# Optimization experiments

Measured on AMD Instinct MI355X. Metric: run time of the kernel, lower is better.

## Reference

```python
import jax, jax.numpy as jnp
import numpy as np
import math

L = 4      # layers / experts
AD = 512   # agent dim per layer
D = 512    # wsi_size / model dim
T = 64     # num_tokens
N = 4096   # WSI patches
NC = 2
PROJ = 256 # cosine gate projection dim
HID = 4 * D
CAP = math.ceil(T / L)  # top-1, capacity_factor=1.0
EPS = 1e-5
AUX_W = 0.01


def layer_norm(x, g, b):
    x32 = x.astype(jnp.float32)
    mu = x32.mean(-1, keepdims=True)
    var = x32.var(-1, keepdims=True)
    return ((x32 - mu) * jax.lax.rsqrt(var + EPS) * g + b).astype(x.dtype)


def mha(q_in, kv_in, w_qkv, b_qkv, w_out, b_out, n_heads):
    # torch nn.MultiheadAttention, unbatched (len, embed) inputs
    E = q_in.shape[-1]
    hd = E // n_heads
    wq, wk, wv = jnp.split(w_qkv, 3, axis=0)
    bq, bk, bv = jnp.split(b_qkv, 3)
    q = (q_in @ wq.T + bq).reshape(-1, n_heads, hd)
    k = (kv_in @ wk.T + bk).reshape(-1, n_heads, hd)
    v = (kv_in @ wv.T + bv).reshape(-1, n_heads, hd)
    scale = float(1.0 / np.sqrt(hd))
    attn = jax.nn.softmax(jnp.einsum('thd,shd->hts', q, k) * scale, axis=-1)
    out = jnp.einsum('hts,shd->thd', attn, v).reshape(-1, E)
    return out @ w_out.T + b_out


def moe_top1(x, proj_w, sim_mat, temp, w1, b1, w2, b2):
    # tutel cosine top-1 gate (fp32), capacity-limited batch-prioritized dispatch
    E = w1.shape[0]
    xf = x.astype(jnp.float32)
    p = xf @ proj_w                                             # [T, PROJ]
    p = p / (jnp.linalg.norm(p, axis=-1, keepdims=True) + 1e-8)
    s = sim_mat / (jnp.linalg.norm(sim_mat, axis=0, keepdims=True) + 1e-8)
    scale = jnp.exp(jnp.minimum(temp, jnp.log(jnp.float32(100.0))))
    logits = (p @ s) * scale                                    # [T, E]
    scores = jax.nn.softmax(logits, axis=-1)
    expert = jnp.argmax(logits, axis=-1)                        # [T]
    gate = jnp.take_along_axis(scores, expert[:, None], axis=1)[:, 0]
    # batch prioritized routing: higher-gate tokens claim capacity slots first
    order = jnp.argsort(-gate)
    oh = jax.nn.one_hot(expert[order], E, dtype=jnp.int32)
    pos_s = jnp.sum(jnp.cumsum(oh, axis=0) * oh, axis=1) - 1    # slot within expert
    inv = jnp.argsort(order)
    pos = pos_s[inv]
    keep = pos < CAP
    safe_pos = jnp.where(keep, pos, 0)
    # dispatch -> grouped expert FFN -> combine
    buf = jnp.zeros((E, CAP, x.shape[-1]), x.dtype)
    buf = buf.at[expert, safe_pos].add(jnp.where(keep[:, None], x, 0.0))
    h = jax.nn.gelu(jnp.einsum('ecd,edh->ech', buf, w1) + b1[:, None, :], approximate=False)
    y = jnp.einsum('ech,ehd->ecd', h, w2) + b2[:, None, :]
    out = y[expert, safe_pos] * (gate * keep)[:, None].astype(x.dtype)
    # load-balancing aux loss (top-1)
    me = scores.mean(0)
    ce = jax.nn.one_hot(expert, E, dtype=jnp.float32).mean(0)
    l_aux = jnp.sum(me * ce) * E
    return out, l_aux


def reference(share_feature, fet_tokens, ind_ln1_g, ind_ln1_b, ind_ln2_g, ind_ln2_b,
              ind_qkv_w, ind_qkv_b, ind_out_w, ind_out_b, ind_mlp_w, ind_mlp_b,
              gate_proj_w, gate_sim, gate_temp, exp_w1, exp_b1, exp_w2, exp_b2,
              gsa_ln1_g, gsa_ln1_b, gsa_qkv_w, gsa_qkv_b, gsa_out_w, gsa_out_b,
              gsa_ln2_g, gsa_ln2_b, gsa_fc_w, gsa_fc_b, gsa_proj_w, gsa_proj_b,
              butter_w, butter_b, cls_w, cls_b):
    cur = jnp.zeros((T, D), share_feature.dtype)
    feature1 = jnp.zeros((L, T, D), share_feature.dtype)
    aux = jnp.zeros((1,), jnp.float32)
    for i in range(L):  # small fixed per-layer loop (structurally distinct params)
        seg = share_feature[:, i * AD:(i + 1) * AD]
        sf = layer_norm(seg, ind_ln1_g[i], ind_ln1_b[i])
        tok = layer_norm(fet_tokens[i], ind_ln2_g[i], ind_ln2_b[i])
        attn_out = mha(tok, sf, ind_qkv_w[i], ind_qkv_b[i], ind_out_w[i], ind_out_b[i], AD)
        qf = attn_out @ ind_mlp_w[i].T + ind_mlp_b[i]   # [T, D]
        mo, la = moe_top1(qf, gate_proj_w, gate_sim, gate_temp, exp_w1, exp_b1, exp_w2, exp_b2)
        cur = cur + mo
        aux = aux + la * AUX_W
        feature1 = feature1.at[i].set(cur)
    cur = cur / L
    # GatedSFAttentionBlock (8 heads self-attn + QuickGELU MLP, pre-LN residual)
    x1 = layer_norm(cur, gsa_ln1_g, gsa_ln1_b)
    x = cur + mha(x1, x1, gsa_qkv_w, gsa_qkv_b, gsa_out_w, gsa_out_b, D // 64)
    x2 = layer_norm(x, gsa_ln2_g, gsa_ln2_b)
    h = x2 @ gsa_fc_w.T + gsa_fc_b
    h = h * jax.nn.sigmoid(1.702 * h)  # QuickGELU
    gated = x + (h @ gsa_proj_w.T + gsa_proj_b)
    # OutputBlock
    hb = (gated @ butter_w.T + butter_b).reshape(1, -1)  # [1, T*256]
    logits = hb @ cls_w.T + cls_b                        # [1, NC]
    Y_hat = jnp.argmax(logits, axis=1, keepdims=True)
    hazards = jax.nn.sigmoid(logits)
    feature2 = jnp.zeros((L, T, D), share_feature.dtype)
    feature2_pre = jnp.zeros((L, 1, NC), share_feature.dtype)
    return (logits, hazards, Y_hat, aux, feature1, feature2, feature2_pre)


def setup_inputs() -> dict:
    key = jax.random.key(0)
    ks = iter(jax.random.split(key, 40))
    def rn(shape, scale=0.02):
        return scale * jax.random.normal(next(ks), shape, dtype=jnp.float32)
    return dict(
        share_feature=jax.random.normal(next(ks), (N, L * AD), dtype=jnp.float32),
        fet_tokens=rn((L, T, AD), AD ** -0.5),
        ind_ln1_g=jnp.ones((L, AD)), ind_ln1_b=jnp.zeros((L, AD)),
        ind_ln2_g=jnp.ones((L, AD)), ind_ln2_b=jnp.zeros((L, AD)),
        ind_qkv_w=rn((L, 3 * AD, AD)), ind_qkv_b=jnp.zeros((L, 3 * AD)),
        ind_out_w=rn((L, AD, AD)), ind_out_b=jnp.zeros((L, AD)),
        ind_mlp_w=rn((L, D, AD)), ind_mlp_b=jnp.zeros((L, D)),
        gate_proj_w=rn((D, PROJ)), gate_sim=rn((PROJ, L)),
        gate_temp=jnp.asarray(np.log(10.0), jnp.float32),
        exp_w1=rn((L, D, HID)), exp_b1=jnp.zeros((L, HID)),
        exp_w2=rn((L, HID, D)), exp_b2=jnp.zeros((L, D)),
        gsa_ln1_g=jnp.ones((D,)), gsa_ln1_b=jnp.zeros((D,)),
        gsa_qkv_w=rn((3 * D, D)), gsa_qkv_b=jnp.zeros((3 * D,)),
        gsa_out_w=rn((D, D)), gsa_out_b=jnp.zeros((D,)),
        gsa_ln2_g=jnp.ones((D,)), gsa_ln2_b=jnp.zeros((D,)),
        gsa_fc_w=rn((4 * D, D)), gsa_fc_b=jnp.zeros((4 * D,)),
        gsa_proj_w=rn((D, 4 * D)), gsa_proj_b=jnp.zeros((D,)),
        butter_w=rn((256, D)), butter_b=jnp.zeros((256,)),
        cls_w=rn((NC, T * 256)), cls_b=jnp.zeros((NC,)),
    )
```

## Files before the change

### kernel.cpp

```cpp
#include <hip/hip_runtime.h>
#include <math.h>

#define LNUM 4
#define ADIM 512
#define TTOK 64
#define NSEQ 4096
#define HIDE 2048
#define CAPE 16
#define EPSV 1e-5f

typedef __bf16 bf16;
typedef bf16 bf16x8 __attribute__((ext_vector_type(8)));
typedef float f32x4 __attribute__((ext_vector_type(4)));

#define OFF_BUF   0
#define OFF_SSUM  (OFF_BUF  + 131072)
#define OFF_CNT   (OFF_SSUM + 16)
#define OFF_Q     (OFF_CNT  + 16)
#define OFF_AP    (OFF_Q    + 131072)
#define OFF_QF    (OFF_AP   + 131072)
#define OFF_P     (OFF_QF   + 131072)
#define OFF_QKV3  (OFF_P    + 65536)
#define OFF_XB    (OFF_QKV3 + 98304)
#define OFF_HROW  (OFF_XB   + 32768)
#define OFF_GTD   (OFF_HROW + 131072)
#define OFF_HB    (OFF_GTD  + 32768)
#define ZERO_N    (OFF_HB   + 16384)
#define OFF_KT    ZERO_N
#define OFF_VT    (OFF_KT   + LNUM*512*NSEQ)
#define OFF_AO    (OFF_VT   + LNUM*512*NSEQ)
#define OFF_GATE  (OFF_AO   + 131072)
#define OFF_EXP   (OFF_GATE + 256)
#define OFF_POS   (OFF_EXP  + 256)
#define OFF_KEEP  (OFF_POS  + 256)
#define OFF_HEXP  (OFF_KEEP + 256)
#define OFF_CUR   (OFF_HEXP + LNUM*4*CAPE*HIDE)
#define OFF_AO2   (OFF_CUR  + TTOK*512)
#define OFF_AH    (OFF_AO2  + TTOK*512)
#define OFF_AL    (OFF_AH + LNUM*NSEQ*256)
#define OFF_WH    (OFF_AL + LNUM*NSEQ*256)
#define OFF_WL    (OFF_WH + LNUM*1024*256)
#define OFF_YEXP  OFF_AH

#define O_F1   6
#define O_F2   (6 + LNUM*TTOK*512)
#define O_F2P  (O_F2 + LNUM*TTOK*512)

__device__ __forceinline__ float wave_sum(float v) {
#pragma unroll
  for (int o = 32; o > 0; o >>= 1) v += __shfl_down(v, o, 64);
  return v;
}
__device__ __forceinline__ float wave_sum_all(float v) {
#pragma unroll
  for (int o = 32; o > 0; o >>= 1) v += __shfl_xor(v, o, 64);
  return v;
}
__device__ __forceinline__ float block_sum256(float v) {
  __shared__ float r[4];
  v = wave_sum(v);
  int wid = threadIdx.x >> 6, lane = threadIdx.x & 63;
  if (lane == 0) r[wid] = v;
  __syncthreads();
  float s = r[0] + r[1] + r[2] + r[3];
  __syncthreads();
  return s;
}

__global__ void k_zero(float* __restrict__ p, int n) {
  int i = blockIdx.x * 256 + threadIdx.x;
  if (i < n) p[i] = 0.f;
}

__global__ __launch_bounds__(64) void k_cvt_a(const float* __restrict__ SF,
      const float* __restrict__ G, const float* __restrict__ Bta,
      bf16* __restrict__ AH, bf16* __restrict__ AL) {
  int row = blockIdx.x;
  int l = row >> 12, m = row & 4095;
  int lane = threadIdx.x;
  const float* src = SF + (size_t)m * (LNUM * ADIM) + l * ADIM;
  float4 a = *(const float4*)(src + lane * 8);
  float4 b = *(const float4*)(src + lane * 8 + 4);
  float sum = (a.x + a.y) + (a.z + a.w) + (b.x + b.y) + (b.z + b.w);
  float sq = a.x*a.x + a.y*a.y + a.z*a.z + a.w*a.w + b.x*b.x + b.y*b.y + b.z*b.z + b.w*b.w;
  sum = wave_sum_all(sum); sq = wave_sum_all(sq);
  float mu = sum * (1.f / 512.f);
  float rs = rsqrtf(sq * (1.f / 512.f) - mu * mu + EPSV);
  float4 g0 = *(const float4*)(G + l * 512 + lane * 8);
  float4 g1 = *(const float4*)(G + l * 512 + lane * 8 + 4);
  float4 c0 = *(const float4*)(Bta + l * 512 + lane * 8);
  float4 c1 = *(const float4*)(Bta + l * 512 + lane * 8 + 4);
  float x[8];
  x[0] = (a.x - mu) * rs * g0.x + c0.x;  x[1] = (a.y - mu) * rs * g0.y + c0.y;
  x[2] = (a.z - mu) * rs * g0.z + c0.z;  x[3] = (a.w - mu) * rs * g0.w + c0.w;
  x[4] = (b.x - mu) * rs * g1.x + c1.x;  x[5] = (b.y - mu) * rs * g1.y + c1.y;
  x[6] = (b.z - mu) * rs * g1.z + c1.z;  x[7] = (b.w - mu) * rs * g1.w + c1.w;
  bf16x8 vh, vl;
#pragma unroll
  for (int j = 0; j < 8; j++) {
    bf16 h = (bf16)x[j];
    vh[j] = h;
    vl[j] = (bf16)(x[j] - (float)h);
  }
  *(bf16x8*)(AH + (size_t)row * 512 + lane * 8) = vh;
  *(bf16x8*)(AL + (size_t)row * 512 + lane * 8) = vl;
}

__global__ __launch_bounds__(64) void k_cvt_w(const float* __restrict__ Wqkv,
      bf16* __restrict__ WH, bf16* __restrict__ WL) {
  int row = blockIdx.x;
  int l = row >> 10, r = row & 1023;
  int lane = threadIdx.x;
  const float* src = Wqkv + (size_t)l * 1536 * 512 + (size_t)(512 + r) * 512 + lane * 8;
  float4 a = *(const float4*)(src);
  float4 b = *(const float4*)(src + 4);
  float x[8] = {a.x, a.y, a.z, a.w, b.x, b.y, b.z, b.w};
  bf16x8 vh, vl;
#pragma unroll
  for (int j = 0; j < 8; j++) {
    bf16 h = (bf16)x[j];
    vh[j] = h;
    vl[j] = (bf16)(x[j] - (float)h);
  }
  *(bf16x8*)(WH + (size_t)row * 512 + lane * 8) = vh;
  *(bf16x8*)(WL + (size_t)row * 512 + lane * 8) = vl;
}

#define KVP 40
__global__ __launch_bounds__(256) void k_mfma_kv(
      const bf16* __restrict__ AH, const bf16* __restrict__ AL,
      const bf16* __restrict__ WH, const bf16* __restrict__ WL,
      const float* __restrict__ Bqkv,
      float* __restrict__ KT, float* __restrict__ VT) {
  __shared__ bf16 sAh[128*KVP], sAl[128*KVP], sWh[128*KVP], sWl[128*KVP];
  int l = blockIdx.z;
  int m0 = blockIdx.x * 128, n0 = blockIdx.y * 128;
  int tid = threadIdx.x;
  int lane = tid & 63;
  int w = tid >> 6;
  int wm = w >> 1, wn = w & 1;
  const bf16* gAh = AH + ((size_t)l * 4096 + m0) * 512;
  const bf16* gAl = AL + ((size_t)l * 4096 + m0) * 512;
  const bf16* gWh = WH + ((size_t)l * 1024 + n0) * 512;
  const bf16* gWl = WL + ((size_t)l * 1024 + n0) * 512;
  int ch0 = tid * 2, ch1 = tid * 2 + 1;
  int r0 = ch0 >> 2, q0 = (ch0 & 3) * 8;
  int r1 = ch1 >> 2, q1 = (ch1 & 3) * 8;
  int fr = lane & 15, fq = (lane >> 4) * 8;
  f32x4 acc[4][4] = {};
  for (int k0 = 0; k0 < 512; k0 += 32) {
    *(bf16x8*)&sAh[r0*KVP + q0] = *(const bf16x8*)&gAh[(size_t)r0*512 + k0 + q0];
    *(bf16x8*)&sAh[r1*KVP + q1] = *(const bf16x8*)&gAh[(size_t)r1*512 + k0 + q1];
    *(bf16x8*)&sAl[r0*KVP + q0] = *(const bf16x8*)&gAl[(size_t)r0*512 + k0 + q0];
    *(bf16x8*)&sAl[r1*KVP + q1] = *(const bf16x8*)&gAl[(size_t)r1*512 + k0 + q1];
    *(bf16x8*)&sWh[r0*KVP + q0] = *(const bf16x8*)&gWh[(size_t)r0*512 + k0 + q0];
    *(bf16x8*)&sWh[r1*KVP + q1] = *(const bf16x8*)&gWh[(size_t)r1*512 + k0 + q1];
    *(bf16x8*)&sWl[r0*KVP + q0] = *(const bf16x8*)&gWl[(size_t)r0*512 + k0 + q0];
    *(bf16x8*)&sWl[r1*KVP + q1] = *(const bf16x8*)&gWl[(size_t)r1*512 + k0 + q1];
    __syncthreads();
    bf16x8 ah[4], al[4], bh[4], bl[4];
#pragma unroll
    for (int i = 0; i < 4; i++) {
      ah[i] = *(const bf16x8*)&sAh[(wm*64 + i*16 + fr)*KVP + fq];
      al[i] = *(const bf16x8*)&sAl[(wm*64 + i*16 + fr)*KVP + fq];
      bh[i] = *(const bf16x8*)&sWh[(wn*64 + i*16 + fr)*KVP + fq];
      bl[i] = *(const bf16x8*)&sWl[(wn*64 + i*16 + fr)*KVP + fq];
    }
#pragma unroll
    for (int i = 0; i < 4; i++)
#pragma unroll
      for (int j = 0; j < 4; j++) {
        acc[i][j] = __builtin_amdgcn_mfma_f32_16x16x32_bf16(ah[i], bh[j], acc[i][j], 0, 0, 0);
        acc[i][j] = __builtin_amdgcn_mfma_f32_16x16x32_bf16(ah[i], bl[j], acc[i][j], 0, 0, 0);
        acc[i][j] = __builtin_amdgcn_mfma_f32_16x16x32_bf16(al[i], bh[j], acc[i][j], 0, 0, 0);
      }
    __syncthreads();
  }
#pragma unroll
  for (int j = 0; j < 4; j++) {
    int n = n0 + wn*64 + j*16 + fr;
    float bias = Bqkv[l * 1536 + 512 + n];
    float* base = (n < 512) ? (KT + ((size_t)(l*512 + n)) * 4096)
                            : (VT + ((size_t)(l*512 + n - 512)) * 4096);
#pragma unroll
    for (int i = 0; i < 4; i++) {
      int mb = m0 + wm*64 + i*16 + (lane >> 4) * 4;
      float4 o = make_float4(acc[i][j][0] + bias, acc[i][j][1] + bias,
                             acc[i][j][2] + bias, acc[i][j][3] + bias);
      *(float4*)(base + mb) = o;
    }
  }
}

__global__ __launch_bounds__(64) void k_ln(const float* __restrict__ IN,
      const float* __restrict__ G, const float* __restrict__ B,
      float* __restrict__ OUT, int gstride) {
  int t = blockIdx.x, l = blockIdx.y;
  int row = l * 64 + t;
  int lane = threadIdx.x;
  const float* x = IN + (size_t)row * 512 + lane * 8;
  float4 a = ((const float4*)x)[0], b = ((const float4*)x)[1];
  float sum = (a.x + a.y) + (a.z + a.w) + (b.x + b.y) + (b.z + b.w);
  float sq = a.x*a.x + a.y*a.y + a.z*a.z + a.w*a.w + b.x*b.x + b.y*b.y + b.z*b.z + b.w*b.w;
  sum = wave_sum_all(sum); sq = wave_sum_all(sq);
  float mu = sum * (1.f / 512.f);
  float rs = rsqrtf(sq * (1.f / 512.f) - mu * mu + EPSV);
  const float* gp = G + l * gstride + lane * 8;
  const float* bp = B + l * gstride + lane * 8;
  float4 g0 = ((const float4*)gp)[0], g1 = ((const float4*)gp)[1];
  float4 c0 = ((const float4*)bp)[0], c1 = ((const float4*)bp)[1];
  float4 o0, o1;
  o0.x = (a.x - mu) * rs * g0.x + c0.x;  o0.y = (a.y - mu) * rs * g0.y + c0.y;
  o0.z = (a.z - mu) * rs * g0.z + c0.z;  o0.w = (a.w - mu) * rs * g0.w + c0.w;
  o1.x = (b.x - mu) * rs * g1.x + c1.x;  o1.y = (b.y - mu) * rs * g1.y + c1.y;
  o1.z = (b.z - mu) * rs * g1.z + c1.z;  o1.w = (b.w - mu) * rs * g1.w + c1.w;
  float* op = OUT + (size_t)row * 512 + lane * 8;
  ((float4*)op)[0] = o0; ((float4*)op)[1] = o1;
}

__global__ __launch_bounds__(256) void k_gemm64(
      const float* __restrict__ IN, const float* __restrict__ W,
      const float* __restrict__ BIAS, const float* __restrict__ RES,
      float* __restrict__ OUT, int K, int N, long wl, int bl, int act) {
  int l = blockIdx.z;
  int n0 = blockIdx.x * 64;
  bool split = (gridDim.y > 1);
  int kcBeg = blockIdx.y * 128;
  int kcEnd = split ? kcBeg + 128 : K;
  const float* INl = IN + (size_t)l * 64 * K;
  const float* Wl  = W + (size_t)l * wl;
  float* OUTl = OUT + (size_t)l * 64 * N;
  __shared__ float sA[64][68], sB[64][68];
  int tid = threadIdx.x;
  int tx = tid & 15, ty = tid >> 4;
  float acc[4][4];
  if (blockIdx.y == 0) {
#pragma unroll
    for (int j = 0; j < 4; j++) {
      float bv = BIAS ? BIAS[bl * l + n0 + tx*4 + j] : 0.f;
#pragma unroll
      for (int i = 0; i < 4; i++)
        acc[i][j] = bv + (RES ? RES[((size_t)l*64 + ty*4 + i) * N + n0 + tx*4 + j] : 0.f);
    }
  } else {
#pragma unroll
    for (int i = 0; i < 4; i++)
#pragma unroll
      for (int j = 0; j < 4; j++) acc[i][j] = 0.f;
  }
  for (int kc = kcBeg; kc < kcEnd; kc += 64) {
    for (int i = tid; i < 1024; i += 256) {
      int r = i >> 4;
      int kq = i & 15;
      float4 av = *(const float4*)(INl + (size_t)r * K + kc + kq*4);
      sA[kq*4+0][r] = av.x; sA[kq*4+1][r] = av.y; sA[kq*4+2][r] = av.z; sA[kq*4+3][r] = av.w;
      float4 bv = *(const float4*)(Wl + (size_t)(n0 + r) * K + kc + kq*4);
      sB[kq*4+0][r] = bv.x; sB[kq*4+1][r] = bv.y; sB[kq*4+2][r] = bv.z; sB[kq*4+3][r] = bv.w;
    }
    __syncthreads();
#pragma unroll 8
    for (int kk = 0; kk < 64; kk++) {
      float4 a4 = *(const float4*)&sA[kk][ty*4];
      float4 b4 = *(const float4*)&sB[kk][tx*4];
      float a[4] = {a4.x,a4.y,a4.z,a4.w}, b[4] = {b4.x,b4.y,b4.z,b4.w};
#pragma unroll
      for (int i = 0; i < 4; i++)
#pragma unroll
        for (int j = 0; j < 4; j++) acc[i][j] = fmaf(a[i], b[j], acc[i][j]);
    }
    __syncthreads();
  }
  if (split) {
#pragma unroll
    for (int i = 0; i < 4; i++)
#pragma unroll
      for (int j = 0; j < 4; j++)
        atomicAdd(&OUTl[(size_t)(ty*4+i) * N + n0 + tx*4 + j], acc[i][j]);
  } else {
#pragma unroll
    for (int i = 0; i < 4; i++)
#pragma unroll
      for (int j = 0; j < 4; j++) {
        float o = acc[i][j];
        if (act == 1) o = o / (1.f + __expf(-1.702f * o));
        OUTl[(size_t)(ty*4+i) * N + n0 + tx*4 + j] = o;
      }
  }
}

__global__ __launch_bounds__(256) void k_gemm64t(
      const float* __restrict__ IN, const float* __restrict__ W,
      float* __restrict__ OUT, int K, int N) {
  int l = blockIdx.z;
  int n0 = blockIdx.x * 64;
  int kc0 = blockIdx.y * 128;
  const float* INl = IN + (size_t)l * 64 * K;
  float* OUTl = OUT + (size_t)l * 64 * N;
  __shared__ float sA[64][68], sB[64][68];
  int tid = threadIdx.x;
  int tx = tid & 15, ty = tid >> 4;
  float acc[4][4] = {};
  for (int kc = kc0; kc < kc0 + 128; kc += 64) {
    for (int i = tid; i < 1024; i += 256) {
      int r = i >> 4;
      int kq = i & 15;
      float4 av = *(const float4*)(INl + (size_t)r * K + kc + kq*4);
      sA[kq*4+0][r] = av.x; sA[kq*4+1][r] = av.y; sA[kq*4+2][r] = av.z; sA[kq*4+3][r] = av.w;
      float4 bv = *(const float4*)(W + (size_t)(kc + r) * N + n0 + kq*4);
      *(float4*)&sB[r][kq*4] = bv;
    }
    __syncthreads();
#pragma unroll 8
    for (int kk = 0; kk < 64; kk++) {
      float4 a4 = *(const float4*)&sA[kk][ty*4];
      float4 b4 = *(const float4*)&sB[kk][tx*4];
      float a[4] = {a4.x,a4.y,a4.z,a4.w}, b[4] = {b4.x,b4.y,b4.z,b4.w};
#pragma unroll
      for (int i = 0; i < 4; i++)
#pragma unroll
        for (int j = 0; j < 4; j++) acc[i][j] = fmaf(a[i], b[j], acc[i][j]);
    }
    __syncthreads();
  }
#pragma unroll
  for (int i = 0; i < 4; i++)
#pragma unroll
    for (int j = 0; j < 4; j++)
      atomicAdd(&OUTl[(size_t)(ty*4+i) * N + n0 + tx*4 + j], acc[i][j]);
}

__global__ __launch_bounds__(256) void k_attn(const float* __restrict__ KT, const float* __restrict__ VT,
      const float* __restrict__ Q, float* __restrict__ AO) {
  int h = blockIdx.x, l = blockIdx.y;
  int tid = threadIdx.x;
  int w = tid >> 6, lane = tid & 63;
  __shared__ float2 sacc[4][8][66];
  __shared__ float wmx[4], wmn[4];
  size_t base = ((size_t)(l * 512 + h)) * 4096 + w * 1024;
  float kv[16], vv[16];
#pragma unroll
  for (int c = 0; c < 4; c++) {
    *(float4*)&kv[c*4] = *(const float4*)(KT + base + c * 256 + lane * 4);
    *(float4*)&vv[c*4] = *(const float4*)(VT + base + c * 256 + lane * 4);
  }
  float mx = kv[0], mn = kv[0];
#pragma unroll
  for (int i = 1; i < 16; i++) { mx = fmaxf(mx, kv[i]); mn = fminf(mn, kv[i]); }
#pragma unroll
  for (int o = 32; o > 0; o >>= 1) {
    mx = fmaxf(mx, __shfl_xor(mx, o, 64));
    mn = fminf(mn, __shfl_xor(mn, o, 64));
  }
  if (lane == 0) { wmx[w] = mx; wmn[w] = mn; }
  __syncthreads();
  float km = fmaxf(fmaxf(wmx[0], wmx[1]), fmaxf(wmx[2], wmx[3]));
  float kn = fminf(fminf(wmn[0], wmn[1]), fminf(wmn[2], wmn[3]));
  float q_own = Q[((size_t)l * TTOK + lane) * 512 + h];
  float m_own = (q_own >= 0.f) ? q_own * km : q_own * kn;
  int rt = tid >> 5, rj = tid & 31;
  for (int cc = 0; cc < 8; cc++) {
    for (int tt = 0; tt < 8; tt++) {
      int t = cc * 8 + tt;
      float qt = __shfl(q_own, t, 64);
      float mt = __shfl(m_own, t, 64);
      float den = 0.f, num = 0.f;
#pragma unroll
      for (int i = 0; i < 16; i++) {
        float e = __expf(fmaf(qt, kv[i], -mt));
        den += e;
        num = fmaf(e, vv[i], num);
      }
      sacc[w][tt][lane] = make_float2(den, num);
    }
    __syncthreads();
    float2 a = make_float2(0.f, 0.f);
#pragma unroll
    for (int g = 0; g < 4; g++)
#pragma unroll
      for (int s2 = 0; s2 < 2; s2++) {
        float2 v = sacc[g][rt][rj + 32 * s2];
        a.x += v.x; a.y += v.y;
      }
#pragma unroll
    for (int o = 16; o > 0; o >>= 1) {
      a.x += __shfl_down(a.x, o, 32);
      a.y += __shfl_down(a.y, o, 32);
    }
    if (rj == 0) {
      int t = cc * 8 + rt;
      AO[((size_t)l * TTOK + t) * 512 + h] = a.y / a.x;
    }
    __syncthreads();
  }
}

__global__ __launch_bounds__(256) void k_moe_gate(const float* __restrict__ P,
      const float* __restrict__ SIM, const float* __restrict__ TEMP,
      const float* __restrict__ QF,
      float* __restrict__ gate, int* __restrict__ expert,
      int* __restrict__ pos, int* __restrict__ keep,
      float* __restrict__ ssum, int* __restrict__ cnt, float* __restrict__ buf) {
  int l = blockIdx.x;
  int tid = threadIdx.x;
  int t = tid >> 2, q = tid & 3;
  __shared__ float score_s[4][64];
  __shared__ float g_s[64];
  __shared__ int e_s[64], keep_s[64], pos_s[64];
  const float* prow = P + ((size_t)(l * 64 + t)) * 256 + q * 64;
  float ss = 0.f, le[4] = {}, ne[4] = {};
  for (int j = 0; j < 64; j++) {
    float pv = prow[j];
    ss = fmaf(pv, pv, ss);
    float4 s4 = *(const float4*)(SIM + (size_t)(q * 64 + j) * 4);
    le[0] = fmaf(pv, s4.x, le[0]); le[1] = fmaf(pv, s4.y, le[1]);
    le[2] = fmaf(pv, s4.z, le[2]); le[3] = fmaf(pv, s4.w, le[3]);
    ne[0] = fmaf(s4.x, s4.x, ne[0]); ne[1] = fmaf(s4.y, s4.y, ne[1]);
    ne[2] = fmaf(s4.z, s4.z, ne[2]); ne[3] = fmaf(s4.w, s4.w, ne[3]);
  }
#pragma unroll
  for (int o = 2; o > 0; o >>= 1) {
    ss += __shfl_xor(ss, o, 4);
#pragma unroll
    for (int e = 0; e < 4; e++) { le[e] += __shfl_xor(le[e], o, 4); ne[e] += __shfl_xor(ne[e], o, 4); }
  }
  if (q == 0) {
    float invp = 1.f / (sqrtf(ss) + 1e-8f);
    float scale = __expf(fminf(TEMP[0], 4.6051701859880914f));
    float lg[4];
#pragma unroll
    for (int e = 0; e < 4; e++) lg[e] = le[e] * invp / (sqrtf(ne[e]) + 1e-8f) * scale;
    int best = 0; float bv = lg[0];
    if (lg[1] > bv) { best = 1; bv = lg[1]; }
    if (lg[2] > bv) { best = 2; bv = lg[2]; }
    if (lg[3] > bv) { best = 3; bv = lg[3]; }
    float mx = fmaxf(fmaxf(lg[0], lg[1]), fmaxf(lg[2], lg[3]));
    float e0 = __expf(lg[0]-mx), e1 = __expf(lg[1]-mx), e2 = __expf(lg[2]-mx), e3 = __expf(lg[3]-mx);
    float inv = 1.f / (e0 + e1 + e2 + e3);
    score_s[0][t] = e0*inv; score_s[1][t] = e1*inv; score_s[2][t] = e2*inv; score_s[3][t] = e3*inv;
    float sb = score_s[best][t];
    g_s[t] = sb; e_s[t] = best;
    gate[l * TTOK + t] = sb;
    expert[l * TTOK + t] = best;
  }
  __syncthreads();
  if (tid < 64) {
    float gt = g_s[tid]; int et = e_s[tid];
    int p = 0;
    for (int u = 0; u < 64; u++)
      if (e_s[u] == et && (g_s[u] > gt || (g_s[u] == gt && u < tid))) p++;
    pos_s[tid] = p; keep_s[tid] = (p < CAPE) ? 1 : 0;
    pos[l * TTOK + tid] = p;
    keep[l * TTOK + tid] = (p < CAPE) ? 1 : 0;
  } else if (tid < 68) {
    int e = tid - 64;
    float s = 0.f; int c = 0;
    for (int u = 0; u < 64; u++) { s += score_s[e][u]; c += (e_s[u] == e); }
    ssum[l * 4 + e] = s;
    cnt[l * 4 + e] = c;
  }
  __syncthreads();
  int which = tid >> 7, idx = tid & 127;
  for (int tb = 0; tb < 64; tb += 2) {
    int tt = tb + which;
    if (keep_s[tt]) {
      float4* dst = (float4*)(buf + (((size_t)(l * 4 + e_s[tt])) * CAPE + pos_s[tt]) * 512);
      dst[idx] = ((const float4*)(QF + ((size_t)l * TTOK + tt) * 512))[idx];
    }
  }
}

__global__ __launch_bounds__(256) void k_moe_h(const float* __restrict__ buf, const float* __restrict__ W1,
      const float* __restrict__ B1, float* __restrict__ H) {
  int le = blockIdx.y;
  int e = le & 3;
  int col = blockIdx.x * 256 + threadIdx.x;
  const float* act = buf + (size_t)le * 16 * 512;
  const float* wp = W1 + (size_t)e * 512 * HIDE + col;
  float acc[16];
#pragma unroll
  for (int c = 0; c < 16; c++) acc[c] = 0.f;
  for (int k0 = 0; k0 < 512; k0 += 4) {
    float4 a[16];
#pragma unroll
    for (int c = 0; c < 16; c++) a[c] = *(const float4*)(act + c * 512 + k0);
#pragma unroll
    for (int j = 0; j < 4; j++) {
      float wv = wp[(size_t)(k0 + j) * HIDE];
#pragma unroll
      for (int c = 0; c < 16; c++) acc[c] = fmaf(((const float*)&a[c])[j], wv, acc[c]);
    }
  }
  float bias = B1[e * HIDE + col];
  float* outp = H + (size_t)le * 16 * HIDE + col;
#pragma unroll
  for (int c = 0; c < 16; c++) {
    float v = acc[c] + bias;
    outp[(size_t)c * HIDE] = 0.5f * v * (1.f + erff(v * 0.70710678118654752f));
  }
}

__global__ __launch_bounds__(256) void k_moe_y(const float* __restrict__ H, const float* __restrict__ W2,
      const float* __restrict__ B2, float* __restrict__ Y) {
  int le = blockIdx.y;
  int e = le & 3;
  int cl = threadIdx.x & 63, kq = threadIdx.x >> 6;
  int col = blockIdx.x * 64 + cl;
  const float* act = H + (size_t)le * 16 * HIDE + kq * 512;
  const float* wp = W2 + (size_t)e * HIDE * 512 + (size_t)(kq * 512) * 512 + col;
  float acc[16];
#pragma unroll
  for (int c = 0; c < 16; c++) acc[c] = 0.f;
  for (int k0 = 0; k0 < 512; k0 += 4) {
    float4 a[16];
#pragma unroll
    for (int c = 0; c < 16; c++) a[c] = *(const float4*)(act + c * HIDE + k0);
#pragma unroll
    for (int j = 0; j < 4; j++) {
      float wv = wp[(size_t)(k0 + j) * 512];
#pragma unroll
      for (int c = 0; c < 16; c++) acc[c] = fmaf(((const float*)&a[c])[j], wv, acc[c]);
    }
  }
  __shared__ float sacc[4][16][64];
#pragma unroll
  for (int c = 0; c < 16; c++) sacc[kq][c][cl] = acc[c];
  __syncthreads();
  if (kq == 0) {
    float bias = B2[e * 512 + col];
#pragma unroll
    for (int c = 0; c < 16; c++) {
      float tot = sacc[0][c][cl] + sacc[1][c][cl] + sacc[2][c][cl] + sacc[3][c][cl] + bias;
      Y[(size_t)le * 16 * 512 + (size_t)c * 512 + col] = tot;
    }
  }
}

__global__ __launch_bounds__(512) void k_combine(const float* __restrict__ Y, const int* __restrict__ expert,
      const int* __restrict__ pos, const int* __restrict__ keep, const float* __restrict__ gate,
      float* __restrict__ f1, float* __restrict__ f2, float* __restrict__ cur) {
  int t = blockIdx.x;
  int d = threadIdx.x;
  float acc = 0.f;
#pragma unroll
  for (int l = 0; l < LNUM; l++) {
    int idx = l * TTOK + t;
    float v = 0.f;
    if (keep[idx]) {
      int e = expert[idx], p = pos[idx];
      v = Y[(((size_t)(l * 4 + e)) * CAPE + p) * 512 + d] * gate[idx];
    }
    acc += v;
    f1[((size_t)l * TTOK + t) * 512 + d] = acc;
    f2[((size_t)l * TTOK + t) * 512 + d] = 0.f;
  }
  cur[(size_t)t * 512 + d] = acc * 0.25f;
}

__global__ __launch_bounds__(256) void k_gsa_attn(const float* __restrict__ QKV3, float* __restrict__ AO2) {
  int h = blockIdx.x;
  __shared__ float qh[64][65], kh[64][65], vh[64][65];
  __shared__ float ps[4][64];
  for (int i = threadIdx.x; i < 4096; i += 256) {
    int t = i >> 6, d = i & 63;
    qh[t][d] = QKV3[(size_t)t * 1536 + h * 64 + d];
    kh[t][d] = QKV3[(size_t)t * 1536 + 512 + h * 64 + d];
    vh[t][d] = QKV3[(size_t)t * 1536 + 1024 + h * 64 + d];
  }
  __syncthreads();
  int w = threadIdx.x >> 6, lane = threadIdx.x & 63;
  for (int tt = 0; tt < 16; tt++) {
    int t = w * 16 + tt;
    float acc = 0.f;
#pragma unroll 8
    for (int d = 0; d < 64; d++) acc = fmaf(qh[t][d], kh[lane][d], acc);
    acc *= 0.125f;
    float m = acc;
#pragma unroll
    for (int o = 32; o > 0; o >>= 1) m = fmaxf(m, __shfl_xor(m, o, 64));
    float e = __expf(acc - m);
    float den = e;
#pragma unroll
    for (int o = 32; o > 0; o >>= 1) den += __shfl_xor(den, o, 64);
    ps[w][lane] = e / den;
    __syncthreads();
    float o2 = 0.f;
#pragma unroll 8
    for (int s = 0; s < 64; s++) o2 = fmaf(ps[w][s], vh[s][lane], o2);
    AO2[(size_t)t * 512 + h * 64 + lane] = o2;
    __syncthreads();
  }
}

__global__ __launch_bounds__(256) void k_final(const float* __restrict__ HB,
      const float* __restrict__ CW, const float* __restrict__ CB,
      const float* __restrict__ ssum, const int* __restrict__ cnt,
      float* __restrict__ out) {
  int tid = threadIdx.x;
  float p0 = 0.f, p1 = 0.f;
  for (int i = tid; i < 16384; i += 256) {
    float h = HB[i];
    p0 = fmaf(h, CW[i], p0);
    p1 = fmaf(h, CW[16384 + i], p1);
  }
  p0 = block_sum256(p0);
  p1 = block_sum256(p1);
  if (tid == 0) {
    float l0 = p0 + CB[0], l1 = p1 + CB[1];
    out[0] = l0; out[1] = l1;
    out[2] = 1.f / (1.f + __expf(-l0));
    out[3] = 1.f / (1.f + __expf(-l1));
    out[4] = (l1 > l0) ? 1.f : 0.f;
    float aux = 0.f;
    for (int i = 0; i < 16; i++) aux += (ssum[i] * (1.f / 64.f)) * ((float)cnt[i] * (1.f / 64.f));
    out[5] = aux * 4.f * 0.01f;
  }
  if (tid < 8) out[O_F2P + tid] = 0.f;
}

extern "C" void kernel_launch(void* const* d_in, const int* in_sizes, int n_in,
                              void* d_out, int out_size, void* d_ws, size_t ws_size,
                              hipStream_t stream) {
  const float* SF    = (const float*)d_in[0];
  const float* TOK   = (const float*)d_in[1];
  const float* LN1G  = (const float*)d_in[2];
  const float* LN1B  = (const float*)d_in[3];
  const float* LN2G  = (const float*)d_in[4];
  const float* LN2B  = (const float*)d_in[5];
  const float* QKVW  = (const float*)d_in[6];
  const float* QKVB  = (const float*)d_in[7];
  const float* OUTW  = (const float*)d_in[8];
  const float* OUTB  = (const float*)d_in[9];
  const float* MLPW  = (const float*)d_in[10];
  const float* MLPB  = (const float*)d_in[11];
  const float* GPW   = (const float*)d_in[12];
  const float* GSIM  = (const float*)d_in[13];
  const float* GTMP  = (const float*)d_in[14];
  const float* EW1   = (const float*)d_in[15];
  const float* EB1   = (const float*)d_in[16];
  const float* EW2   = (const float*)d_in[17];
  const float* EB2   = (const float*)d_in[18];
  const float* GL1G  = (const float*)d_in[19];
  const float* GL1B  = (const float*)d_in[20];
  const float* GQKVW = (const float*)d_in[21];
  const float* GQKVB = (const float*)d_in[22];
  const float* GOUTW = (const float*)d_in[23];
  const float* GOUTB = (const float*)d_in[24];
  const float* GL2G  = (const float*)d_in[25];
  const float* GL2B  = (const float*)d_in[26];
  const float* GFCW  = (const float*)d_in[27];
  const float* GFCB  = (const float*)d_in[28];
  const float* GPJW  = (const float*)d_in[29];
  const float* GPJB  = (const float*)d_in[30];
  const float* BTW   = (const float*)d_in[31];
  const float* BTB   = (const float*)d_in[32];
  const float* CLW   = (const float*)d_in[33];
  const float* CLB   = (const float*)d_in[34];

  float* ws  = (float*)d_ws;
  float* out = (float*)d_out;

  float* BUF  = ws + OFF_BUF;
  float* SSUM = ws + OFF_SSUM;
  int*   CNT  = (int*)(ws + OFF_CNT);
  float* Q    = ws + OFF_Q;
  float* AP   = ws + OFF_AP;
  float* QF   = ws + OFF_QF;
  float* P    = ws + OFF_P;
  float* QKV3 = ws + OFF_QKV3;
  float* XB   = ws + OFF_XB;
  float* HROW = ws + OFF_HROW;
  float* GTD  = ws + OFF_GTD;
  float* HBB  = ws + OFF_HB;
  float* KT   = ws + OFF_KT;
  float* VT   = ws + OFF_VT;
  float* AOSH = ws + OFF_AO;
  float* GATE = ws + OFF_GATE;
  int*   EXPI = (int*)(ws + OFF_EXP);
  int*   POSI = (int*)(ws + OFF_POS);
  int*   KEEPI= (int*)(ws + OFF_KEEP);
  float* HEXP = ws + OFF_HEXP;
  float* CUR  = ws + OFF_CUR;
  float* AO2  = ws + OFF_AO2;
  bf16*  AH   = (bf16*)(ws + OFF_AH);
  bf16*  AL   = (bf16*)(ws + OFF_AL);
  bf16*  WH   = (bf16*)(ws + OFF_WH);
  bf16*  WL   = (bf16*)(ws + OFF_WL);
  float* YEXP = ws + OFF_YEXP;

  k_zero<<<(ZERO_N + 255) / 256, 256, 0, stream>>>(ws, ZERO_N);
  k_cvt_a<<<LNUM * NSEQ, 64, 0, stream>>>(SF, LN1G, LN1B, AH, AL);
  k_cvt_w<<<LNUM * 1024, 64, 0, stream>>>(QKVW, WH, WL);
  k_mfma_kv<<<dim3(32, 8, LNUM), 256, 0, stream>>>(AH, AL, WH, WL, QKVB, KT, VT);
  k_ln<<<dim3(TTOK, LNUM), 64, 0, stream>>>(TOK, LN2G, LN2B, AOSH, 512);
  k_gemm64<<<dim3(8, 4, LNUM), 256, 0, stream>>>(AOSH, QKVW, QKVB, nullptr, Q, 512, 512, 1536L*512, 1536, 0);
  k_attn<<<dim3(512, LNUM), 256, 0, stream>>>(KT, VT, Q, AOSH);
  k_gemm64<<<dim3(8, 4, LNUM), 256, 0, stream>>>(AOSH, OUTW, OUTB, nullptr, AP, 512, 512, 512L*512, 512, 0);
  k_gemm64<<<dim3(8, 4, LNUM), 256, 0, stream>>>(AP, MLPW, MLPB, nullptr, QF, 512, 512, 512L*512, 512, 0);
  k_gemm64t<<<dim3(4, 4, LNUM), 256, 0, stream>>>(QF, GPW, P, 512, 256);
  k_moe_gate<<<LNUM, 256, 0, stream>>>(P, GSIM, GTMP, QF, GATE, EXPI, POSI, KEEPI, SSUM, CNT, BUF);
  k_moe_h<<<dim3(8, 16), 256, 0, stream>>>(BUF, EW1, EB1, HEXP);
  k_moe_y<<<dim3(8, 16), 256, 0, stream>>>(HEXP, EW2, EB2, YEXP);
  k_combine<<<TTOK, 512, 0, stream>>>(YEXP, EXPI, POSI, KEEPI, GATE, out + O_F1, out + O_F2, CUR);
  k_ln<<<dim3(TTOK, 1), 64, 0, stream>>>(CUR, GL1G, GL1B, AOSH, 0);
  k_gemm64<<<dim3(24, 4, 1), 256, 0, stream>>>(AOSH, GQKVW, GQKVB, nullptr, QKV3, 512, 1536, 0, 0, 0);
  k_gsa_attn<<<8, 256, 0, stream>>>(QKV3, AO2);
  k_gemm64<<<dim3(8, 4, 1), 256, 0, stream>>>(AO2, GOUTW, GOUTB, CUR, XB, 512, 512, 0, 0, 0);
  k_ln<<<dim3(TTOK, 1), 64, 0, stream>>>(XB, GL2G, GL2B, AOSH, 0);
  k_gemm64<<<dim3(32, 1, 1), 256, 0, stream>>>(AOSH, GFCW, GFCB, nullptr, HROW, 512, 2048, 0, 0, 1);
  k_gemm64<<<dim3(8, 16, 1), 256, 0, stream>>>(HROW, GPJW, GPJB, XB, GTD, 2048, 512, 0, 0, 0);
  k_gemm64<<<dim3(4, 4, 1), 256, 0, stream>>>(GTD, BTW, BTB, nullptr, HBB, 512, 256, 0, 0, 0);
  k_final<<<1, 256, 0, stream>>>(HBB, CLW, CLB, SSUM, CNT, out);
}
```

Baseline: 792.8 us.

## Merge many small kernel launches into persistent megakernels with grid barriers

After: 982.0 us. 23.9% more time.

```diff
diff --git a/kernel.cpp b/kernel.cpp
--- a/kernel.cpp
+++ b/kernel.cpp
@@ -8,15 +8,23 @@
 #define HIDE 2048
 #define CAPE 16
 #define EPSV 1e-5f
+#define LOG2E 1.44269504088896340736f
 
 typedef __bf16 bf16;
 typedef bf16 bf16x8 __attribute__((ext_vector_type(8)));
 typedef float f32x4 __attribute__((ext_vector_type(4)));
 
+#if __has_builtin(__builtin_amdgcn_exp2f)
+#define EXP2F(x) __builtin_amdgcn_exp2f(x)
+#else
+#define EXP2F(x) __expf(0.69314718055994530942f * (x))
+#endif
+
 #define OFF_BUF   0
-#define OFF_SSUM  (OFF_BUF  + 131072)
-#define OFF_CNT   (OFF_SSUM + 16)
-#define OFF_Q     (OFF_CNT  + 16)
+#define OFF_SSUM  131072
+#define OFF_CNT   131088
+#define OFF_BAR   131104
+#define OFF_Q     131120
 #define OFF_AP    (OFF_Q    + 131072)
 #define OFF_QF    (OFF_AP   + 131072)
 #define OFF_P     (OFF_QF   + 131072)
@@ -26,6 +34,7 @@
 #define OFF_GTD   (OFF_HROW + 131072)
 #define OFF_HB    (OFF_GTD  + 32768)
 #define ZERO_N    (OFF_HB   + 16384)
+#define NZB       ((ZERO_N + 255) / 256)
 #define OFF_KT    ZERO_N
 #define OFF_VT    (OFF_KT   + LNUM*512*NSEQ)
 #define OFF_AO    (OFF_VT   + LNUM*512*NSEQ)
@@ -67,180 +76,53 @@
   return s;
 }
 
-__global__ void k_zero(float* __restrict__ p, int n) {
-  int i = blockIdx.x * 256 + threadIdx.x;
-  if (i < n) p[i] = 0.f;
-}
-
-__global__ __launch_bounds__(64) void k_cvt_a(const float* __restrict__ SF,
-      const float* __restrict__ G, const float* __restrict__ Bta,
-      bf16* __restrict__ AH, bf16* __restrict__ AL) {
-  int row = blockIdx.x;
-  int l = row >> 12, m = row & 4095;
-  int lane = threadIdx.x;
-  const float* src = SF + (size_t)m * (LNUM * ADIM) + l * ADIM;
-  float4 a = *(const float4*)(src + lane * 8);
-  float4 b = *(const float4*)(src + lane * 8 + 4);
+__device__ __forceinline__ void gsync(unsigned* bar, unsigned target) {
+  __syncthreads();
+  if (threadIdx.x == 0) {
+    __threadfence();
+    atomicAdd(bar, 1u);
+    while (__hip_atomic_load(bar, __ATOMIC_RELAXED, __HIP_MEMORY_SCOPE_AGENT) < target)
+      __builtin_amdgcn_s_sleep(2);
+  }
+  __syncthreads();
+  __threadfence();
+}
+
+__device__ __forceinline__ void ln_row(const float* __restrict__ x,
+      const float* __restrict__ G, const float* __restrict__ B, float* __restrict__ o) {
+  int lane = threadIdx.x & 63;
+  float4 a = *(const float4*)(x + lane * 8);
+  float4 b = *(const float4*)(x + lane * 8 + 4);
   float sum = (a.x + a.y) + (a.z + a.w) + (b.x + b.y) + (b.z + b.w);
   float sq = a.x*a.x + a.y*a.y + a.z*a.z + a.w*a.w + b.x*b.x + b.y*b.y + b.z*b.z + b.w*b.w;
   sum = wave_sum_all(sum); sq = wave_sum_all(sq);
   float mu = sum * (1.f / 512.f);
   float rs = rsqrtf(sq * (1.f / 512.f) - mu * mu + EPSV);
-  float4 g0 = *(const float4*)(G + l * 512 + lane * 8);
-  float4 g1 = *(const float4*)(G + l * 512 + lane * 8 + 4);
-  float4 c0 = *(const float4*)(Bta + l * 512 + lane * 8);
-  float4 c1 = *(const float4*)(Bta + l * 512 + lane * 8 + 4);
-  float x[8];
-  x[0] = (a.x - mu) * rs * g0.x + c0.x;  x[1] = (a.y - mu) * rs * g0.y + c0.y;
-  x[2] = (a.z - mu) * rs * g0.z + c0.z;  x[3] = (a.w - mu) * rs * g0.w + c0.w;
-  x[4] = (b.x - mu) * rs * g1.x + c1.x;  x[5] = (b.y - mu) * rs * g1.y + c1.y;
-  x[6] = (b.z - mu) * rs * g1.z + c1.z;  x[7] = (b.w - mu) * rs * g1.w + c1.w;
-  bf16x8 vh, vl;
-#pragma unroll
-  for (int j = 0; j < 8; j++) {
-    bf16 h = (bf16)x[j];
-    vh[j] = h;
-    vl[j] = (bf16)(x[j] - (float)h);
-  }
-  *(bf16x8*)(AH + (size_t)row * 512 + lane * 8) = vh;
-  *(bf16x8*)(AL + (size_t)row * 512 + lane * 8) = vl;
-}
-
-__global__ __launch_bounds__(64) void k_cvt_w(const float* __restrict__ Wqkv,
-      bf16* __restrict__ WH, bf16* __restrict__ WL) {
-  int row = blockIdx.x;
-  int l = row >> 10, r = row & 1023;
-  int lane = threadIdx.x;
-  const float* src = Wqkv + (size_t)l * 1536 * 512 + (size_t)(512 + r) * 512 + lane * 8;
-  float4 a = *(const float4*)(src);
-  float4 b = *(const float4*)(src + 4);
-  float x[8] = {a.x, a.y, a.z, a.w, b.x, b.y, b.z, b.w};
-  bf16x8 vh, vl;
-#pragma unroll
-  for (int j = 0; j < 8; j++) {
-    bf16 h = (bf16)x[j];
-    vh[j] = h;
-    vl[j] = (bf16)(x[j] - (float)h);
-  }
-  *(bf16x8*)(WH + (size_t)row * 512 + lane * 8) = vh;
-  *(bf16x8*)(WL + (size_t)row * 512 + lane * 8) = vl;
-}
-
-#define KVP 40
-__global__ __launch_bounds__(256) void k_mfma_kv(
-      const bf16* __restrict__ AH, const bf16* __restrict__ AL,
-      const bf16* __restrict__ WH, const bf16* __restrict__ WL,
-      const float* __restrict__ Bqkv,
-      float* __restrict__ KT, float* __restrict__ VT) {
-  __shared__ bf16 sAh[128*KVP], sAl[128*KVP], sWh[128*KVP], sWl[128*KVP];
-  int l = blockIdx.z;
-  int m0 = blockIdx.x * 128, n0 = blockIdx.y * 128;
-  int tid = threadIdx.x;
-  int lane = tid & 63;
-  int w = tid >> 6;
-  int wm = w >> 1, wn = w & 1;
-  const bf16* gAh = AH + ((size_t)l * 4096 + m0) * 512;
-  const bf16* gAl = AL + ((size_t)l * 4096 + m0) * 512;
-  const bf16* gWh = WH + ((size_t)l * 1024 + n0) * 512;
-  const bf16* gWl = WL + ((size_t)l * 1024 + n0) * 512;
-  int ch0 = tid * 2, ch1 = tid * 2 + 1;
-  int r0 = ch0 >> 2, q0 = (ch0 & 3) * 8;
-  int r1 = ch1 >> 2, q1 = (ch1 & 3) * 8;
-  int fr = lane & 15, fq = (lane >> 4) * 8;
-  f32x4 acc[4][4] = {};
-  for (int k0 = 0; k0 < 512; k0 += 32) {
-    *(bf16x8*)&sAh[r0*KVP + q0] = *(const bf16x8*)&gAh[(size_t)r0*512 + k0 + q0];
-    *(bf16x8*)&sAh[r1*KVP + q1] = *(const bf16x8*)&gAh[(size_t)r1*512 + k0 + q1];
-    *(bf16x8*)&sAl[r0*KVP + q0] = *(const bf16x8*)&gAl[(size_t)r0*512 + k0 + q0];
-    *(bf16x8*)&sAl[r1*KVP + q1] = *(const bf16x8*)&gAl[(size_t)r1*512 + k0 + q1];
-    *(bf16x8*)&sWh[r0*KVP + q0] = *(const bf16x8*)&gWh[(size_t)r0*512 + k0 + q0];
-    *(bf16x8*)&sWh[r1*KVP + q1] = *(const bf16x8*)&gWh[(size_t)r1*512 + k0 + q1];
-    *(bf16x8*)&sWl[r0*KVP + q0] = *(const bf16x8*)&gWl[(size_t)r0*512 + k0 + q0];
-    *(bf16x8*)&sWl[r1*KVP + q1] = *(const bf16x8*)&gWl[(size_t)r1*512 + k0 + q1];
-    __syncthreads();
-    bf16x8 ah[4], al[4], bh[4], bl[4];
-#pragma unroll
-    for (int i = 0; i < 4; i++) {
-      ah[i] = *(const bf16x8*)&sAh[(wm*64 + i*16 + fr)*KVP + fq];
-      al[i] = *(const bf16x8*)&sAl[(wm*64 + i*16 + fr)*KVP + fq];
-      bh[i] = *(const bf16x8*)&sWh[(wn*64 + i*16 + fr)*KVP + fq];
-      bl[i] = *(const bf16x8*)&sWl[(wn*64 + i*16 + fr)*KVP + fq];
-    }
-#pragma unroll
-    for (int i = 0; i < 4; i++)
-#pragma unroll
-      for (int j = 0; j < 4; j++) {
-        acc[i][j] = __builtin_amdgcn_mfma_f32_16x16x32_bf16(ah[i], bh[j], acc[i][j], 0, 0, 0);
-        acc[i][j] = __builtin_amdgcn_mfma_f32_16x16x32_bf16(ah[i], bl[j], acc[i][j], 0, 0, 0);
-        acc[i][j] = __builtin_amdgcn_mfma_f32_16x16x32_bf16(al[i], bh[j], acc[i][j], 0, 0, 0);
-      }
-    __syncthreads();
-  }
-#pragma unroll
-  for (int j = 0; j < 4; j++) {
-    int n = n0 + wn*64 + j*16 + fr;
-    float bias = Bqkv[l * 1536 + 512 + n];
-    float* base = (n < 512) ? (KT + ((size_t)(l*512 + n)) * 4096)
-                            : (VT + ((size_t)(l*512 + n - 512)) * 4096);
-#pragma unroll
-    for (int i = 0; i < 4; i++) {
-      int mb = m0 + wm*64 + i*16 + (lane >> 4) * 4;
-      float4 o = make_float4(acc[i][j][0] + bias, acc[i][j][1] + bias,
-                             acc[i][j][2] + bias, acc[i][j][3] + bias);
-      *(float4*)(base + mb) = o;
-    }
-  }
-}
-
-__global__ __launch_bounds__(64) void k_ln(const float* __restrict__ IN,
-      const float* __restrict__ G, const float* __restrict__ B,
-      float* __restrict__ OUT, int gstride) {
-  int t = blockIdx.x, l = blockIdx.y;
-  int row = l * 64 + t;
-  int lane = threadIdx.x;
-  const float* x = IN + (size_t)row * 512 + lane * 8;
-  float4 a = ((const float4*)x)[0], b = ((const float4*)x)[1];
-  float sum = (a.x + a.y) + (a.z + a.w) + (b.x + b.y) + (b.z + b.w);
-  float sq = a.x*a.x + a.y*a.y + a.z*a.z + a.w*a.w + b.x*b.x + b.y*b.y + b.z*b.z + b.w*b.w;
-  sum = wave_sum_all(sum); sq = wave_sum_all(sq);
-  float mu = sum * (1.f / 512.f);
-  float rs = rsqrtf(sq * (1.f / 512.f) - mu * mu + EPSV);
-  const float* gp = G + l * gstride + lane * 8;
-  const float* bp = B + l * gstride + lane * 8;
-  float4 g0 = ((const float4*)gp)[0], g1 = ((const float4*)gp)[1];
-  float4 c0 = ((const float4*)bp)[0], c1 = ((const float4*)bp)[1];
+  float4 g0 = *(const float4*)(G + lane * 8), g1 = *(const float4*)(G + lane * 8 + 4);
+  float4 c0 = *(const float4*)(B + lane * 8), c1 = *(const float4*)(B + lane * 8 + 4);
   float4 o0, o1;
   o0.x = (a.x - mu) * rs * g0.x + c0.x;  o0.y = (a.y - mu) * rs * g0.y + c0.y;
   o0.z = (a.z - mu) * rs * g0.z + c0.z;  o0.w = (a.w - mu) * rs * g0.w + c0.w;
   o1.x = (b.x - mu) * rs * g1.x + c1.x;  o1.y = (b.y - mu) * rs * g1.y + c1.y;
   o1.z = (b.z - mu) * rs * g1.z + c1.z;  o1.w = (b.w - mu) * rs * g1.w + c1.w;
-  float* op = OUT + (size_t)row * 512 + lane * 8;
-  ((float4*)op)[0] = o0; ((float4*)op)[1] = o1;
-}
-
-__global__ __launch_bounds__(256) void k_gemm64(
-      const float* __restrict__ IN, const float* __restrict__ W,
-      const float* __restrict__ BIAS, const float* __restrict__ RES,
-      float* __restrict__ OUT, int K, int N, long wl, int bl, int act) {
-  int l = blockIdx.z;
-  int n0 = blockIdx.x * 64;
-  bool split = (gridDim.y > 1);
-  int kcBeg = blockIdx.y * 128;
-  int kcEnd = split ? kcBeg + 128 : K;
-  const float* INl = IN + (size_t)l * 64 * K;
-  const float* Wl  = W + (size_t)l * wl;
-  float* OUTl = OUT + (size_t)l * 64 * N;
-  __shared__ float sA[64][68], sB[64][68];
+  *(float4*)(o + lane * 8) = o0; *(float4*)(o + lane * 8 + 4) = o1;
+}
+
+__device__ __forceinline__ void dev_gemm(
+    const float* __restrict__ IN, const float* __restrict__ W,
+    const float* __restrict__ BIAS, const float* __restrict__ RES,
+    float* __restrict__ OUT, int K, int N, int n0, int kcBeg, int kcEnd,
+    int doBias, int doAtomic, int act, float* sA, float* sB) {
   int tid = threadIdx.x;
   int tx = tid & 15, ty = tid >> 4;
   float acc[4][4];
-  if (blockIdx.y == 0) {
+  if (doBias) {
 #pragma unroll
     for (int j = 0; j < 4; j++) {
-      float bv = BIAS ? BIAS[bl * l + n0 + tx*4 + j] : 0.f;
+      float bv = BIAS ? BIAS[n0 + tx*4 + j] : 0.f;
 #pragma unroll
       for (int i = 0; i < 4; i++)
-        acc[i][j] = bv + (RES ? RES[((size_t)l*64 + ty*4 + i) * N + n0 + tx*4 + j] : 0.f);
+        acc[i][j] = bv + (RES ? RES[(size_t)(ty*4+i) * N + n0 + tx*4 + j] : 0.f);
     }
   } else {
 #pragma unroll
@@ -250,18 +132,19 @@
   }
   for (int kc = kcBeg; kc < kcEnd; kc += 64) {
     for (int i = tid; i < 1024; i += 256) {
-      int r = i >> 4;
-      int kq = i & 15;
-      float4 av = *(const float4*)(INl + (size_t)r * K + kc + kq*4);
-      sA[kq*4+0][r] = av.x; sA[kq*4+1][r] = av.y; sA[kq*4+2][r] = av.z; sA[kq*4+3][r] = av.w;
-      float4 bv = *(const float4*)(Wl + (size_t)(n0 + r) * K + kc + kq*4);
-      sB[kq*4+0][r] = bv.x; sB[kq*4+1][r] = bv.y; sB[kq*4+2][r] = bv.z; sB[kq*4+3][r] = bv.w;
+      int r = i >> 4, kq = i & 15;
+      float4 av = *(const float4*)(IN + (size_t)r * K + kc + kq*4);
+      sA[(kq*4+0)*68 + r] = av.x; sA[(kq*4+1)*68 + r] = av.y;
+      sA[(kq*4+2)*68 + r] = av.z; sA[(kq*4+3)*68 + r] = av.w;
+      float4 bv = *(const float4*)(W + (size_t)(n0 + r) * K + kc + kq*4);
+      sB[(kq*4+0)*68 + r] = bv.x; sB[(kq*4+1)*68 + r] = bv.y;
+      sB[(kq*4+2)*68 + r] = bv.z; sB[(kq*4+3)*68 + r] = bv.w;
     }
     __syncthreads();
 #pragma unroll 8
     for (int kk = 0; kk < 64; kk++) {
-      float4 a4 = *(const float4*)&sA[kk][ty*4];
-      float4 b4 = *(const float4*)&sB[kk][tx*4];
+      float4 a4 = *(const float4*)&sA[kk*68 + ty*4];
+      float4 b4 = *(const float4*)&sB[kk*68 + tx*4];
       float a[4] = {a4.x,a4.y,a4.z,a4.w}, b[4] = {b4.x,b4.y,b4.z,b4.w};
 #pragma unroll
       for (int i = 0; i < 4; i++)
@@ -270,12 +153,12 @@
     }
     __syncthreads();
   }
-  if (split) {
+  if (doAtomic) {
 #pragma unroll
     for (int i = 0; i < 4; i++)
 #pragma unroll
       for (int j = 0; j < 4; j++)
-        atomicAdd(&OUTl[(size_t)(ty*4+i) * N + n0 + tx*4 + j], acc[i][j]);
+        atomicAdd(&OUT[(size_t)(ty*4+i) * N + n0 + tx*4 + j], acc[i][j]);
   } else {
 #pragma unroll
     for (int i = 0; i < 4; i++)
@@ -283,37 +166,32 @@
       for (int j = 0; j < 4; j++) {
         float o = acc[i][j];
         if (act == 1) o = o / (1.f + __expf(-1.702f * o));
-        OUTl[(size_t)(ty*4+i) * N + n0 + tx*4 + j] = o;
-      }
-  }
-}
-
-__global__ __launch_bounds__(256) void k_gemm64t(
-      const float* __restrict__ IN, const float* __restrict__ W,
-      float* __restrict__ OUT, int K, int N) {
-  int l = blockIdx.z;
-  int n0 = blockIdx.x * 64;
-  int kc0 = blockIdx.y * 128;
-  const float* INl = IN + (size_t)l * 64 * K;
-  float* OUTl = OUT + (size_t)l * 64 * N;
-  __shared__ float sA[64][68], sB[64][68];
+        OUT[(size_t)(ty*4+i) * N + n0 + tx*4 + j] = o;
+      }
+  }
+}
+
+__device__ __forceinline__ void dev_gemmt(
+    const float* __restrict__ IN, const float* __restrict__ W,
+    float* __restrict__ OUT, int K, int N, int n0, int kcBeg, int kcEnd,
+    float* sA, float* sB) {
   int tid = threadIdx.x;
   int tx = tid & 15, ty = tid >> 4;
   float acc[4][4] = {};
-  for (int kc = kc0; kc < kc0 + 128; kc += 64) {
+  for (int kc = kcBeg; kc < kcEnd; kc += 64) {
     for (int i = tid; i < 1024; i += 256) {
-      int r = i >> 4;
-      int kq = i & 15;
-      float4 av = *(const float4*)(INl + (size_t)r * K + kc + kq*4);
-      sA[kq*4+0][r] = av.x; sA[kq*4+1][r] = av.y; sA[kq*4+2][r] = av.z; sA[kq*4+3][r] = av.w;
+      int r = i >> 4, kq = i & 15;
+      float4 av = *(const float4*)(IN + (size_t)r * K + kc + kq*4);
+      sA[(kq*4+0)*68 + r] = av.x; sA[(kq*4+1)*68 + r] = av.y;
+      sA[(kq*4+2)*68 + r] = av.z; sA[(kq*4+3)*68 + r] = av.w;
       float4 bv = *(const float4*)(W + (size_t)(kc + r) * N + n0 + kq*4);
-      *(float4*)&sB[r][kq*4] = bv;
+      *(float4*)&sB[r*68 + kq*4] = bv;
     }
     __syncthreads();
 #pragma unroll 8
     for (int kk = 0; kk < 64; kk++) {
-      float4 a4 = *(const float4*)&sA[kk][ty*4];
-      float4 b4 = *(const float4*)&sB[kk][tx*4];
+      float4 a4 = *(const float4*)&sA[kk*68 + ty*4];
+      float4 b4 = *(const float4*)&sB[kk*68 + tx*4];
       float a[4] = {a4.x,a4.y,a4.z,a4.w}, b[4] = {b4.x,b4.y,b4.z,b4.w};
 #pragma unroll
       for (int i = 0; i < 4; i++)
@@ -326,7 +204,162 @@
   for (int i = 0; i < 4; i++)
 #pragma unroll
     for (int j = 0; j < 4; j++)
-      atomicAdd(&OUTl[(size_t)(ty*4+i) * N + n0 + tx*4 + j], acc[i][j]);
+      atomicAdd(&OUT[(size_t)(ty*4+i) * N + n0 + tx*4 + j], acc[i][j]);
+}
+
+__global__ __launch_bounds__(256) void k_mega1(
+    const float* __restrict__ SF, const float* __restrict__ LN1G, const float* __restrict__ LN1B,
+    const float* __restrict__ Wqkv, const float* __restrict__ TOK,
+    const float* __restrict__ LN2G, const float* __restrict__ LN2B,
+    bf16* __restrict__ AH, bf16* __restrict__ AL,
+    bf16* __restrict__ WH, bf16* __restrict__ WL,
+    float* __restrict__ XN, float* __restrict__ ws) {
+  int bid = blockIdx.x, tid = threadIdx.x;
+  if (bid < NZB) {
+    int i = bid * 256 + tid;
+    if (i < ZERO_N) ws[i] = 0.f;
+    return;
+  }
+  bid -= NZB;
+  int wave = tid >> 6, lane = tid & 63;
+  if (bid < 4096) {
+    int row = bid * 4 + wave;
+    int l = row >> 12, m = row & 4095;
+    const float* src = SF + (size_t)m * (LNUM * ADIM) + l * ADIM;
+    float4 a = *(const float4*)(src + lane * 8);
+    float4 b = *(const float4*)(src + lane * 8 + 4);
+    float sum = (a.x + a.y) + (a.z + a.w) + (b.x + b.y) + (b.z + b.w);
+    float sq = a.x*a.x + a.y*a.y + a.z*a.z + a.w*a.w + b.x*b.x + b.y*b.y + b.z*b.z + b.w*b.w;
+    sum = wave_sum_all(sum); sq = wave_sum_all(sq);
+    float mu = sum * (1.f / 512.f);
+    float rs = rsqrtf(sq * (1.f / 512.f) - mu * mu + EPSV);
+    float4 g0 = *(const float4*)(LN1G + l * 512 + lane * 8);
+    float4 g1 = *(const float4*)(LN1G + l * 512 + lane * 8 + 4);
+    float4 c0 = *(const float4*)(LN1B + l * 512 + lane * 8);
+    float4 c1 = *(const float4*)(LN1B + l * 512 + lane * 8 + 4);
+    float x[8];
+    x[0] = (a.x - mu) * rs * g0.x + c0.x;  x[1] = (a.y - mu) * rs * g0.y + c0.y;
+    x[2] = (a.z - mu) * rs * g0.z + c0.z;  x[3] = (a.w - mu) * rs * g0.w + c0.w;
+    x[4] = (b.x - mu) * rs * g1.x + c1.x;  x[5] = (b.y - mu) * rs * g1.y + c1.y;
+    x[6] = (b.z - mu) * rs * g1.z + c1.z;  x[7] = (b.w - mu) * rs * g1.w + c1.w;
+    bf16x8 vh, vl;
+#pragma unroll
+    for (int j = 0; j < 8; j++) {
+      bf16 h = (bf16)x[j];
+      vh[j] = h;
+      vl[j] = (bf16)(x[j] - (float)h);
+    }
+    *(bf16x8*)(AH + (size_t)row * 512 + lane * 8) = vh;
+    *(bf16x8*)(AL + (size_t)row * 512 + lane * 8) = vl;
+    return;
+  }
+  bid -= 4096;
+  if (bid < 1024) {
+    int row = bid * 4 + wave;
+    int l = row >> 10, r = row & 1023;
+    const float* src = Wqkv + (size_t)l * 1536 * 512 + (size_t)(512 + r) * 512 + lane * 8;
+    float4 a = *(const float4*)(src);
+    float4 b = *(const float4*)(src + 4);
+    float x[8] = {a.x, a.y, a.z, a.w, b.x, b.y, b.z, b.w};
+    bf16x8 vh, vl;
+#pragma unroll
+    for (int j = 0; j < 8; j++) {
+      bf16 h = (bf16)x[j];
+      vh[j] = h;
+      vl[j] = (bf16)(x[j] - (float)h);
+    }
+    *(bf16x8*)(WH + (size_t)row * 512 + lane * 8) = vh;
+    *(bf16x8*)(WL + (size_t)row * 512 + lane * 8) = vl;
+    return;
+  }
+  bid -= 1024;
+  {
+    int row = bid * 4 + wave;
+    int l = row >> 6;
+    ln_row(TOK + (size_t)row * 512, LN2G + l * 512, LN2B + l * 512, XN + (size_t)row * 512);
+  }
+}
+
+#define KVP 40
+__global__ __launch_bounds__(256) void k_l2(
+    const bf16* __restrict__ AH, const bf16* __restrict__ AL,
+    const bf16* __restrict__ WH, const bf16* __restrict__ WL,
+    const float* __restrict__ Bqkv, const float* __restrict__ Wqkv,
+    const float* __restrict__ XN,
+    float* __restrict__ KT, float* __restrict__ VT, float* __restrict__ Q) {
+  __shared__ char smem[4 * 128 * KVP * sizeof(bf16)];
+  int bid = blockIdx.x;
+  int tid = threadIdx.x;
+  if (bid < 1024) {
+    bf16* sAh = (bf16*)smem;
+    bf16* sAl = sAh + 128 * KVP;
+    bf16* sWh = sAl + 128 * KVP;
+    bf16* sWl = sWh + 128 * KVP;
+    int l = bid >> 8, rem = bid & 255;
+    int n0 = (rem >> 5) * 128, m0 = (rem & 31) * 128;
+    int lane = tid & 63;
+    int w = tid >> 6;
+    int wm = w >> 1, wn = w & 1;
+    const bf16* gAh = AH + ((size_t)l * 4096 + m0) * 512;
+    const bf16* gAl = AL + ((size_t)l * 4096 + m0) * 512;
+    const bf16* gWh = WH + ((size_t)l * 1024 + n0) * 512;
+    const bf16* gWl = WL + ((size_t)l * 1024 + n0) * 512;
+    int ch0 = tid * 2, ch1 = tid * 2 + 1;
+    int r0 = ch0 >> 2, q0 = (ch0 & 3) * 8;
+    int r1 = ch1 >> 2, q1 = (ch1 & 3) * 8;
+    int fr = lane & 15, fq = (lane >> 4) * 8;
+    f32x4 acc[4][4] = {};
+    for (int k0 = 0; k0 < 512; k0 += 32) {
+      *(bf16x8*)&sAh[r0*KVP + q0] = *(const bf16x8*)&gAh[(size_t)r0*512 + k0 + q0];
+      *(bf16x8*)&sAh[r1*KVP + q1] = *(const bf16x8*)&gAh[(size_t)r1*512 + k0 + q1];
+      *(bf16x8*)&sAl[r0*KVP + q0] = *(const bf16x8*)&gAl[(size_t)r0*512 + k0 + q0];
+      *(bf16x8*)&sAl[r1*KVP + q1] = *(const bf16x8*)&gAl[(size_t)r1*512 + k0 + q1];
+      *(bf16x8*)&sWh[r0*KVP + q0] = *(const bf16x8*)&gWh[(size_t)r0*512 + k0 + q0];
+      *(bf16x8*)&sWh[r1*KVP + q1] = *(const bf16x8*)&gWh[(size_t)r1*512 + k0 + q1];
+      *(bf16x8*)&sWl[r0*KVP + q0] = *(const bf16x8*)&gWl[(size_t)r0*512 + k0 + q0];
+      *(bf16x8*)&sWl[r1*KVP + q1] = *(const bf16x8*)&gWl[(size_t)r1*512 + k0 + q1];
+      __syncthreads();
+      bf16x8 ah[4], al[4], bh[4], bl[4];
+#pragma unroll
+      for (int i = 0; i < 4; i++) {
+        ah[i] = *(const bf16x8*)&sAh[(wm*64 + i*16 + fr)*KVP + fq];
+        al[i] = *(const bf16x8*)&sAl[(wm*64 + i*16 + fr)*KVP + fq];
+        bh[i] = *(const bf16x8*)&sWh[(wn*64 + i*16 + fr)*KVP + fq];
+        bl[i] = *(const bf16x8*)&sWl[(wn*64 + i*16 + fr)*KVP + fq];
+      }
+#pragma unroll
+      for (int i = 0; i < 4; i++)
+#pragma unroll
+        for (int j = 0; j < 4; j++) {
+          acc[i][j] = __builtin_amdgcn_mfma_f32_16x16x32_bf16(ah[i], bh[j], acc[i][j], 0, 0, 0);
+          acc[i][j] = __builtin_amdgcn_mfma_f32_16x16x32_bf16(ah[i], bl[j], acc[i][j], 0, 0, 0);
+          acc[i][j] = __builtin_amdgcn_mfma_f32_16x16x32_bf16(al[i], bh[j], acc[i][j], 0, 0, 0);
+        }
+      __syncthreads();
+    }
+#pragma unroll
+    for (int j = 0; j < 4; j++) {
+      int n = n0 + wn*64 + j*16 + fr;
+      float bias = Bqkv[l * 1536 + 512 + n];
+      float* base = (n < 512) ? (KT + ((size_t)(l*512 + n)) * 4096)
+                              : (VT + ((size_t)(l*512 + n - 512)) * 4096);
+#pragma unroll
+      for (int i = 0; i < 4; i++) {
+        int mb = m0 + wm*64 + i*16 + (lane >> 4) * 4;
+        float4 o = make_float4(acc[i][j][0] + bias, acc[i][j][1] + bias,
+                               acc[i][j][2] + bias, acc[i][j][3] + bias);
+        *(float4*)(base + mb) = o;
+      }
+    }
+  } else {
+    float* sA = (float*)smem;
+    float* sB = sA + 64 * 68;
+    int rem = bid - 1024;
+    int l = rem >> 5, r2 = rem & 31, kcb = r2 >> 3, nb = r2 & 7;
+    dev_gemm(XN + (size_t)l * 64 * 512, Wqkv + (size_t)l * 1536 * 512,
+             Bqkv + l * 1536, nullptr, Q + (size_t)l * 64 * 512,
+             512, 512, nb * 64, kcb * 128, kcb * 128 + 128, kcb == 0, 1, 0, sA, sB);
+  }
 }
 
 __global__ __launch_bounds__(256) void k_attn(const float* __restrict__ KT, const float* __restrict__ VT,
@@ -356,17 +389,18 @@
   float km = fmaxf(fmaxf(wmx[0], wmx[1]), fmaxf(wmx[2], wmx[3]));
   float kn = fminf(fminf(wmn[0], wmn[1]), fminf(wmn[2], wmn[3]));
   float q_own = Q[((size_t)l * TTOK + lane) * 512 + h];
-  float m_own = (q_own >= 0.f) ? q_own * km : q_own * kn;
+  float q2_own = q_own * LOG2E;
+  float m2_own = ((q_own >= 0.f) ? q_own * km : q_own * kn) * LOG2E;
   int rt = tid >> 5, rj = tid & 31;
   for (int cc = 0; cc < 8; cc++) {
     for (int tt = 0; tt < 8; tt++) {
       int t = cc * 8 + tt;
-      float qt = __shfl(q_own, t, 64);
-      float mt = __shfl(m_own, t, 64);
+      float q2t = __shfl(q2_own, t, 64);
+      float m2t = __shfl(m2_own, t, 64);
       float den = 0.f, num = 0.f;
 #pragma unroll
       for (int i = 0; i < 16; i++) {
-        float e = __expf(fmaf(qt, kv[i], -mt));
+        float e = EXP2F(fmaf(q2t, kv[i], -m2t));
         den += e;
         num = fmaf(e, vv[i], num);
       }
@@ -394,227 +428,307 @@
   }
 }
 
-__global__ __launch_bounds__(256) void k_moe_gate(const float* __restrict__ P,
-      const float* __restrict__ SIM, const float* __restrict__ TEMP,
-      const float* __restrict__ QF,
-      float* __restrict__ gate, int* __restrict__ expert,
-      int* __restrict__ pos, int* __restrict__ keep,
-      float* __restrict__ ssum, int* __restrict__ cnt, float* __restrict__ buf) {
-  int l = blockIdx.x;
+__global__ __launch_bounds__(256) void k_mega2(
+    const float* __restrict__ AO, const float* __restrict__ OUTW, const float* __restrict__ OUTB,
+    float* __restrict__ AP, const float* __restrict__ MLPW, const float* __restrict__ MLPB,
+    float* __restrict__ QF, const float* __restrict__ GPW, float* __restrict__ P,
+    const float* __restrict__ SIM, const float* __restrict__ TEMP,
+    float* __restrict__ GATE, int* __restrict__ EXPI, int* __restrict__ POSI, int* __restrict__ KEEPI,
+    float* __restrict__ SSUM, int* __restrict__ CNT, float* __restrict__ BUF,
+    const float* __restrict__ EW1, const float* __restrict__ EB1, float* __restrict__ HEXP,
+    const float* __restrict__ EW2, const float* __restrict__ EB2, float* __restrict__ YEXP,
+    float* __restrict__ f1, float* __restrict__ f2, float* __restrict__ CUR,
+    unsigned* __restrict__ bar) {
+  __shared__ float smem[8704];
+  float* sA = smem;
+  float* sB = smem + 64 * 68;
+  int bid = blockIdx.x;
   int tid = threadIdx.x;
-  int t = tid >> 2, q = tid & 3;
-  __shared__ float score_s[4][64];
-  __shared__ float g_s[64];
-  __shared__ int e_s[64], keep_s[64], pos_s[64];
-  const float* prow = P + ((size_t)(l * 64 + t)) * 256 + q * 64;
-  float ss = 0.f, le[4] = {}, ne[4] = {};
-  for (int j = 0; j < 64; j++) {
-    float pv = prow[j];
-    ss = fmaf(pv, pv, ss);
-    float4 s4 = *(const float4*)(SIM + (size_t)(q * 64 + j) * 4);
-    le[0] = fmaf(pv, s4.x, le[0]); le[1] = fmaf(pv, s4.y, le[1]);
-    le[2] = fmaf(pv, s4.z, le[2]); le[3] = fmaf(pv, s4.w, le[3]);
-    ne[0] = fmaf(s4.x, s4.x, ne[0]); ne[1] = fmaf(s4.y, s4.y, ne[1]);
-    ne[2] = fmaf(s4.z, s4.z, ne[2]); ne[3] = fmaf(s4.w, s4.w, ne[3]);
-  }
-#pragma unroll
-  for (int o = 2; o > 0; o >>= 1) {
-    ss += __shfl_xor(ss, o, 4);
-#pragma unroll
-    for (int e = 0; e < 4; e++) { le[e] += __shfl_xor(le[e], o, 4); ne[e] += __shfl_xor(ne[e], o, 4); }
-  }
-  if (q == 0) {
-    float invp = 1.f / (sqrtf(ss) + 1e-8f);
-    float scale = __expf(fminf(TEMP[0], 4.6051701859880914f));
-    float lg[4];
-#pragma unroll
-    for (int e = 0; e < 4; e++) lg[e] = le[e] * invp / (sqrtf(ne[e]) + 1e-8f) * scale;
-    int best = 0; float bv = lg[0];
-    if (lg[1] > bv) { best = 1; bv = lg[1]; }
-    if (lg[2] > bv) { best = 2; bv = lg[2]; }
-    if (lg[3] > bv) { best = 3; bv = lg[3]; }
-    float mx = fmaxf(fmaxf(lg[0], lg[1]), fmaxf(lg[2], lg[3]));
-    float e0 = __expf(lg[0]-mx), e1 = __expf(lg[1]-mx), e2 = __expf(lg[2]-mx), e3 = __expf(lg[3]-mx);
-    float inv = 1.f / (e0 + e1 + e2 + e3);
-    score_s[0][t] = e0*inv; score_s[1][t] = e1*inv; score_s[2][t] = e2*inv; score_s[3][t] = e3*inv;
-    float sb = score_s[best][t];
-    g_s[t] = sb; e_s[t] = best;
-    gate[l * TTOK + t] = sb;
-    expert[l * TTOK + t] = best;
-  }
-  __syncthreads();
-  if (tid < 64) {
-    float gt = g_s[tid]; int et = e_s[tid];
-    int p = 0;
-    for (int u = 0; u < 64; u++)
-      if (e_s[u] == et && (g_s[u] > gt || (g_s[u] == gt && u < tid))) p++;
-    pos_s[tid] = p; keep_s[tid] = (p < CAPE) ? 1 : 0;
-    pos[l * TTOK + tid] = p;
-    keep[l * TTOK + tid] = (p < CAPE) ? 1 : 0;
-  } else if (tid < 68) {
-    int e = tid - 64;
-    float s = 0.f; int c = 0;
-    for (int u = 0; u < 64; u++) { s += score_s[e][u]; c += (e_s[u] == e); }
-    ssum[l * 4 + e] = s;
-    cnt[l * 4 + e] = c;
-  }
-  __syncthreads();
-  int which = tid >> 7, idx = tid & 127;
-  for (int tb = 0; tb < 64; tb += 2) {
-    int tt = tb + which;
-    if (keep_s[tt]) {
-      float4* dst = (float4*)(buf + (((size_t)(l * 4 + e_s[tt])) * CAPE + pos_s[tt]) * 512);
-      dst[idx] = ((const float4*)(QF + ((size_t)l * TTOK + tt) * 512))[idx];
-    }
-  }
-}
-
-__global__ __launch_bounds__(256) void k_moe_h(const float* __restrict__ buf, const float* __restrict__ W1,
-      const float* __restrict__ B1, float* __restrict__ H) {
-  int le = blockIdx.y;
-  int e = le & 3;
-  int col = blockIdx.x * 256 + threadIdx.x;
-  const float* act = buf + (size_t)le * 16 * 512;
-  const float* wp = W1 + (size_t)e * 512 * HIDE + col;
-  float acc[16];
-#pragma unroll
-  for (int c = 0; c < 16; c++) acc[c] = 0.f;
-  for (int k0 = 0; k0 < 512; k0 += 4) {
-    float4 a[16];
-#pragma unroll
-    for (int c = 0; c < 16; c++) a[c] = *(const float4*)(act + c * 512 + k0);
-#pragma unroll
-    for (int j = 0; j < 4; j++) {
-      float wv = wp[(size_t)(k0 + j) * HIDE];
-#pragma unroll
-      for (int c = 0; c < 16; c++) acc[c] = fmaf(((const float*)&a[c])[j], wv, acc[c]);
-    }
-  }
-  float bias = B1[e * HIDE + col];
-  float* outp = H + (size_t)le * 16 * HIDE + col;
-#pragma unroll
-  for (int c = 0; c < 16; c++) {
-    float v = acc[c] + bias;
-    outp[(size_t)c * HIDE] = 0.5f * v * (1.f + erff(v * 0.70710678118654752f));
-  }
-}
-
-__global__ __launch_bounds__(256) void k_moe_y(const float* __restrict__ H, const float* __restrict__ W2,
-      const float* __restrict__ B2, float* __restrict__ Y) {
-  int le = blockIdx.y;
-  int e = le & 3;
-  int cl = threadIdx.x & 63, kq = threadIdx.x >> 6;
-  int col = blockIdx.x * 64 + cl;
-  const float* act = H + (size_t)le * 16 * HIDE + kq * 512;
-  const float* wp = W2 + (size_t)e * HIDE * 512 + (size_t)(kq * 512) * 512 + col;
-  float acc[16];
-#pragma unroll
-  for (int c = 0; c < 16; c++) acc[c] = 0.f;
-  for (int k0 = 0; k0 < 512; k0 += 4) {
-    float4 a[16];
-#pragma unroll
-    for (int c = 0; c < 16; c++) a[c] = *(const float4*)(act + c * HIDE + k0);
-#pragma unroll
-    for (int j = 0; j < 4; j++) {
-      float wv = wp[(size_t)(k0 + j) * 512];
-#pragma unroll
-      for (int c = 0; c < 16; c++) acc[c] = fmaf(((const float*)&a[c])[j], wv, acc[c]);
-    }
-  }
-  __shared__ float sacc[4][16][64];
-#pragma unroll
-  for (int c = 0; c < 16; c++) sacc[kq][c][cl] = acc[c];
-  __syncthreads();
-  if (kq == 0) {
-    float bias = B2[e * 512 + col];
+  {
+    int l = bid >> 5, r = bid & 31, kcb = r >> 3, nb = r & 7;
+    dev_gemm(AO + (size_t)l*64*512, OUTW + (size_t)l*512*512, OUTB + l*512, nullptr,
+             AP + (size_t)l*64*512, 512, 512, nb*64, kcb*128, kcb*128+128, kcb == 0, 1, 0, sA, sB);
+  }
+  gsync(bar, 128);
+  {
+    int l = bid >> 5, r = bid & 31, kcb = r >> 3, nb = r & 7;
+    dev_gemm(AP + (size_t)l*64*512, MLPW + (size_t)l*512*512, MLPB + l*512, nullptr,
+             QF + (size_t)l*64*512, 512, 512, nb*64, kcb*128, kcb*128+128, kcb == 0, 1, 0, sA, sB);
+  }
+  gsync(bar, 256);
+  if (bid < 64) {
+    int l = bid >> 4, r = bid & 15, kcb = r >> 2, nb = r & 3;
+    dev_gemmt(QF + (size_t)l*64*512, GPW, P + (size_t)l*64*256, 512, 256,
+              nb*64, kcb*128, kcb*128+128, sA, sB);
+  }
+  gsync(bar, 384);
+  if (bid < 4) {
+    int l = bid;
+    int t = tid >> 2, q = tid & 3;
+    float* score_s = smem;
+    float* g_s = smem + 256;
+    int* e_s = (int*)(smem + 320);
+    int* keep_s = e_s + 64;
+    int* pos_s = keep_s + 64;
+    const float* prow = P + ((size_t)(l * 64 + t)) * 256 + q * 64;
+    float ss = 0.f, le[4] = {}, ne[4] = {};
+    for (int j = 0; j < 64; j++) {
+      float pv = prow[j];
+      ss = fmaf(pv, pv, ss);
+      float4 s4 = *(const float4*)(SIM + (size_t)(q * 64 + j) * 4);
+      le[0] = fmaf(pv, s4.x, le[0]); le[1] = fmaf(pv, s4.y, le[1]);
+      le[2] = fmaf(pv, s4.z, le[2]); le[3] = fmaf(pv, s4.w, le[3]);
+      ne[0] = fmaf(s4.x, s4.x, ne[0]); ne[1] = fmaf(s4.y, s4.y, ne[1]);
+      ne[2] = fmaf(s4.z, s4.z, ne[2]); ne[3] = fmaf(s4.w, s4.w, ne[3]);
+    }
+#pragma unroll
+    for (int o = 2; o > 0; o >>= 1) {
+      ss += __shfl_xor(ss, o, 4);
+#pragma unroll
+      for (int e = 0; e < 4; e++) { le[e] += __shfl_xor(le[e], o, 4); ne[e] += __shfl_xor(ne[e], o, 4); }
+    }
+    if (q == 0) {
+      float invp = 1.f / (sqrtf(ss) + 1e-8f);
+      float scale = __expf(fminf(TEMP[0], 4.6051701859880914f));
+      float lg[4];
+#pragma unroll
+      for (int e = 0; e < 4; e++) lg[e] = le[e] * invp / (sqrtf(ne[e]) + 1e-8f) * scale;
+      int best = 0; float bv = lg[0];
+      if (lg[1] > bv) { best = 1; bv = lg[1]; }
+      if (lg[2] > bv) { best = 2; bv = lg[2]; }
+      if (lg[3] > bv) { best = 3; bv = lg[3]; }
+      float mxl = fmaxf(fmaxf(lg[0], lg[1]), fmaxf(lg[2], lg[3]));
+      float e0 = __expf(lg[0]-mxl), e1 = __expf(lg[1]-mxl), e2 = __expf(lg[2]-mxl), e3 = __expf(lg[3]-mxl);
+      float inv = 1.f / (e0 + e1 + e2 + e3);
+      score_s[0*64+t] = e0*inv; score_s[1*64+t] = e1*inv;
+      score_s[2*64+t] = e2*inv; score_s[3*64+t] = e3*inv;
+      float sb = score_s[best*64+t];
+      g_s[t] = sb; e_s[t] = best;
+      GATE[l * TTOK + t] = sb;
+      EXPI[l * TTOK + t] = best;
+    }
+    __syncthreads();
+    if (tid < 64) {
+      float gt = g_s[tid]; int et = e_s[tid];
+      int p = 0;
+      for (int u = 0; u < 64; u++)
+        if (e_s[u] == et && (g_s[u] > gt || (g_s[u] == gt && u < tid))) p++;
+      pos_s[tid] = p; keep_s[tid] = (p < CAPE) ? 1 : 0;
+      POSI[l * TTOK + tid] = p;
+      KEEPI[l * TTOK + tid] = (p < CAPE) ? 1 : 0;
+    } else if (tid < 68) {
+      int e = tid - 64;
+      float s = 0.f; int c = 0;
+      for (int u = 0; u < 64; u++) { s += score_s[e*64+u]; c += (e_s[u] == e); }
+      SSUM[l * 4 + e] = s;
+      CNT[l * 4 + e] = c;
+    }
+    __syncthreads();
+    int which = tid >> 7, idx = tid & 127;
+    for (int tb = 0; tb < 64; tb += 2) {
+      int tt = tb + which;
+      if (keep_s[tt]) {
+        float4* dst = (float4*)(BUF + (((size_t)(l * 4 + e_s[tt])) * CAPE + pos_s[tt]) * 512);
+        dst[idx] = ((const float4*)(QF + ((size_t)l * TTOK + tt) * 512))[idx];
+      }
+    }
+  }
+  gsync(bar, 512);
+  {
+    int le = bid >> 3;
+    int e = le & 3;
+    int col = (bid & 7) * 256 + tid;
+    const float* act = BUF + (size_t)le * 16 * 512;
+    const float* wp = EW1 + (size_t)e * 512 * HIDE + col;
+    float acc[16];
+#pragma unroll
+    for (int c = 0; c < 16; c++) acc[c] = 0.f;
+    for (int k0 = 0; k0 < 512; k0 += 4) {
+      float4 a[16];
+#pragma unroll
+      for (int c = 0; c < 16; c++) a[c] = *(const float4*)(act + c * 512 + k0);
+#pragma unroll
+      for (int j = 0; j < 4; j++) {
+        float wv = wp[(size_t)(k0 + j) * HIDE];
+#pragma unroll
+        for (int c = 0; c < 16; c++) acc[c] = fmaf(((const float*)&a[c])[j], wv, acc[c]);
+      }
+    }
+    float bias = EB1[e * HIDE + col];
+    float* outp = HEXP + (size_t)le * 16 * HIDE + col;
 #pragma unroll
     for (int c = 0; c < 16; c++) {
-      float tot = sacc[0][c][cl] + sacc[1][c][cl] + sacc[2][c][cl] + sacc[3][c][cl] + bias;
-      Y[(size_t)le * 16 * 512 + (size_t)c * 512 + col] = tot;
-    }
-  }
-}
-
-__global__ __launch_bounds__(512) void k_combine(const float* __restrict__ Y, const int* __restrict__ expert,
-      const int* __restrict__ pos, const int* __restrict__ keep, const float* __restrict__ gate,
-      float* __restrict__ f1, float* __restrict__ f2, float* __restrict__ cur) {
-  int t = blockIdx.x;
-  int d = threadIdx.x;
-  float acc = 0.f;
-#pragma unroll
-  for (int l = 0; l < LNUM; l++) {
-    int idx = l * TTOK + t;
-    float v = 0.f;
-    if (keep[idx]) {
-      int e = expert[idx], p = pos[idx];
-      v = Y[(((size_t)(l * 4 + e)) * CAPE + p) * 512 + d] * gate[idx];
-    }
-    acc += v;
-    f1[((size_t)l * TTOK + t) * 512 + d] = acc;
-    f2[((size_t)l * TTOK + t) * 512 + d] = 0.f;
-  }
-  cur[(size_t)t * 512 + d] = acc * 0.25f;
-}
-
-__global__ __launch_bounds__(256) void k_gsa_attn(const float* __restrict__ QKV3, float* __restrict__ AO2) {
-  int h = blockIdx.x;
-  __shared__ float qh[64][65], kh[64][65], vh[64][65];
-  __shared__ float ps[4][64];
-  for (int i = threadIdx.x; i < 4096; i += 256) {
-    int t = i >> 6, d = i & 63;
-    qh[t][d] = QKV3[(size_t)t * 1536 + h * 64 + d];
-    kh[t][d] = QKV3[(size_t)t * 1536 + 512 + h * 64 + d];
-    vh[t][d] = QKV3[(size_t)t * 1536 + 1024 + h * 64 + d];
-  }
-  __syncthreads();
-  int w = threadIdx.x >> 6, lane = threadIdx.x & 63;
-  for (int tt = 0; tt < 16; tt++) {
-    int t = w * 16 + tt;
-    float acc = 0.f;
+      float v = acc[c] + bias;
+      outp[(size_t)c * HIDE] = 0.5f * v * (1.f + erff(v * 0.70710678118654752f));
+    }
+  }
+  gsync(bar, 640);
+  {
+    int le = bid >> 3;
+    int e = le & 3;
+    int cl = tid & 63, kq = tid >> 6;
+    int col = (bid & 7) * 64 + cl;
+    const float* act = HEXP + (size_t)le * 16 * HIDE + kq * 512;
+    const float* wp = EW2 + (size_t)e * HIDE * 512 + (size_t)(kq * 512) * 512 + col;
+    float acc[16];
+#pragma unroll
+    for (int c = 0; c < 16; c++) acc[c] = 0.f;
+    for (int k0 = 0; k0 < 512; k0 += 4) {
+      float4 a[16];
+#pragma unroll
+      for (int c = 0; c < 16; c++) a[c] = *(const float4*)(act + c * HIDE + k0);
+#pragma unroll
+      for (int j = 0; j < 4; j++) {
+        float wv = wp[(size_t)(k0 + j) * 512];
+#pragma unroll
+        for (int c = 0; c < 16; c++) acc[c] = fmaf(((const float*)&a[c])[j], wv, acc[c]);
+      }
+    }
+    float* sacc = smem;
+    __syncthreads();
+#pragma unroll
+    for (int c = 0; c < 16; c++) sacc[(kq*16 + c)*64 + cl] = acc[c];
+    __syncthreads();
+    if (kq == 0) {
+      float bias = EB2[e * 512 + col];
+#pragma unroll
+      for (int c = 0; c < 16; c++) {
+        float tot = sacc[(0*16+c)*64+cl] + sacc[(1*16+c)*64+cl]
+                  + sacc[(2*16+c)*64+cl] + sacc[(3*16+c)*64+cl] + bias;
+        YEXP[(size_t)le * 16 * 512 + (size_t)c * 512 + col] = tot;
+      }
+    }
+  }
+  gsync(bar, 768);
+  if (bid < 64) {
+    int t = bid;
+    int d0 = tid, d1 = tid + 256;
+    float a0 = 0.f, a1 = 0.f;
+#pragma unroll
+    for (int l = 0; l < LNUM; l++) {
+      int idx = l * TTOK + t;
+      if (KEEPI[idx]) {
+        size_t b = (((size_t)(l * 4 + EXPI[idx])) * CAPE + POSI[idx]) * 512;
+        float g = GATE[idx];
+        a0 = fmaf(YEXP[b + d0], g, a0);
+        a1 = fmaf(YEXP[b + d1], g, a1);
+      }
+      size_t r = ((size_t)l * TTOK + t) * 512;
+      f1[r + d0] = a0; f1[r + d1] = a1;
+      f2[r + d0] = 0.f; f2[r + d1] = 0.f;
+    }
+    CUR[(size_t)t * 512 + d0] = a0 * 0.25f;
+    CUR[(size_t)t * 512 + d1] = a1 * 0.25f;
+  }
+}
+
+__global__ __launch_bounds__(256) void k_mega3(
+    const float* __restrict__ CUR, const float* __restrict__ GL1G, const float* __restrict__ GL1B,
+    float* __restrict__ XN, const float* __restrict__ GQKVW, const float* __restrict__ GQKVB,
+    float* __restrict__ QKV3, float* __restrict__ AO2,
+    const float* __restrict__ GOUTW, const float* __restrict__ GOUTB, float* __restrict__ XB,
+    const float* __restrict__ GL2G, const float* __restrict__ GL2B,
+    const float* __restrict__ GFCW, const float* __restrict__ GFCB, float* __restrict__ HROW,
+    const float* __restrict__ GPJW, const float* __restrict__ GPJB, float* __restrict__ GTD,
+    const float* __restrict__ BTW, const float* __restrict__ BTB, float* __restrict__ HBB,
+    const float* __restrict__ CLW, const float* __restrict__ CLB,
+    const float* __restrict__ SSUM, const int* __restrict__ CNT,
+    float* __restrict__ out, unsigned* __restrict__ bar) {
+  __shared__ float smem[12736];
+  float* sA = smem;
+  float* sB = smem + 64 * 68;
+  int bid = blockIdx.x;
+  int tid = threadIdx.x;
+  if (tid < 64) ln_row(CUR + (size_t)bid * 512, GL1G, GL1B, XN + (size_t)bid * 512);
+  gsync(bar, 64);
+  if (bid < 48) {
+    int nb = bid % 24, kcb = bid / 24;
+    dev_gemm(XN, GQKVW, GQKVB, nullptr, QKV3, 512, 1536, nb*64,
+             kcb*256, kcb*256+256, kcb == 0, 1, 0, sA, sB);
+  }
+  gsync(bar, 128);
+  if (bid < 8) {
+    int h = bid;
+    float* qh = smem;
+    float* kh = smem + 4160;
+    float* vh = smem + 8320;
+    float* ps = smem + 12480;
+    __syncthreads();
+    for (int i = tid; i < 4096; i += 256) {
+      int t = i >> 6, d = i & 63;
+      qh[t*65 + d] = QKV3[(size_t)t * 1536 + h * 64 + d];
+      kh[t*65 + d] = QKV3[(size_t)t * 1536 + 512 + h * 64 + d];
+      vh[t*65 + d] = QKV3[(size_t)t * 1536 + 1024 + h * 64 + d];
+    }
+    __syncthreads();
+    int w = tid >> 6, lane = tid & 63;
+    for (int tt = 0; tt < 16; tt++) {
+      int t = w * 16 + tt;
+      float acc = 0.f;
 #pragma unroll 8
-    for (int d = 0; d < 64; d++) acc = fmaf(qh[t][d], kh[lane][d], acc);
-    acc *= 0.125f;
-    float m = acc;
-#pragma unroll
-    for (int o = 32; o > 0; o >>= 1) m = fmaxf(m, __shfl_xor(m, o, 64));
-    float e = __expf(acc - m);
-    float den = e;
-#pragma unroll
-    for (int o = 32; o > 0; o >>= 1) den += __shfl_xor(den, o, 64);
-    ps[w][lane] = e / den;
-    __syncthreads();
-    float o2 = 0.f;
+      for (int d = 0; d < 64; d++) acc = fmaf(qh[t*65 + d], kh[lane*65 + d], acc);
+      acc *= 0.125f;
+      float m = acc;
+#pragma unroll
+      for (int o = 32; o > 0; o >>= 1) m = fmaxf(m, __shfl_xor(m, o, 64));
+      float e = __expf(acc - m);
+      float den = e;
+#pragma unroll
+      for (int o = 32; o > 0; o >>= 1) den += __shfl_xor(den, o, 64);
+      ps[w*64 + lane] = e / den;
+      __syncthreads();
+      float o2 = 0.f;
 #pragma unroll 8
-    for (int s = 0; s < 64; s++) o2 = fmaf(ps[w][s], vh[s][lane], o2);
-    AO2[(size_t)t * 512 + h * 64 + lane] = o2;
-    __syncthreads();
-  }
-}
-
-__global__ __launch_bounds__(256) void k_final(const float* __restrict__ HB,
-      const float* __restrict__ CW, const float* __restrict__ CB,
-      const float* __restrict__ ssum, const int* __restrict__ cnt,
-      float* __restrict__ out) {
-  int tid = threadIdx.x;
-  float p0 = 0.f, p1 = 0.f;
-  for (int i = tid; i < 16384; i += 256) {
-    float h = HB[i];
-    p0 = fmaf(h, CW[i], p0);
-    p1 = fmaf(h, CW[16384 + i], p1);
-  }
-  p0 = block_sum256(p0);
-  p1 = block_sum256(p1);
-  if (tid == 0) {
-    float l0 = p0 + CB[0], l1 = p1 + CB[1];
-    out[0] = l0; out[1] = l1;
-    out[2] = 1.f / (1.f + __expf(-l0));
-    out[3] = 1.f / (1.f + __expf(-l1));
-    out[4] = (l1 > l0) ? 1.f : 0.f;
-    float aux = 0.f;
-    for (int i = 0; i < 16; i++) aux += (ssum[i] * (1.f / 64.f)) * ((float)cnt[i] * (1.f / 64.f));
-    out[5] = aux * 4.f * 0.01f;
-  }
-  if (tid < 8) out[O_F2P + tid] = 0.f;
+      for (int s = 0; s < 64; s++) o2 = fmaf(ps[w*64 + s], vh[s*65 + lane], o2);
+      AO2[(size_t)t * 512 + h * 64 + lane] = o2;
+      __syncthreads();
+    }
+  }
+  gsync(bar, 192);
+  if (bid < 16) {
+    int nb = bid & 7, kcb = bid >> 3;
+    dev_gemm(AO2, GOUTW, GOUTB, CUR, XB, 512, 512, nb*64,
+             kcb*256, kcb*256+256, kcb == 0, 1, 0, sA, sB);
+  }
+  gsync(bar, 256);
+  if (tid < 64) ln_row(XB + (size_t)bid * 512, GL2G, GL2B, XN + (size_t)bid * 512);
+  gsync(bar, 320);
+  if (bid < 32)
+    dev_gemm(XN, GFCW, GFCB, nullptr, HROW, 512, 2048, bid*64, 0, 512, 1, 0, 1, sA, sB);
+  gsync(bar, 384);
+  if (bid < 32) {
+    int nb = bid & 7, kcb = bid >> 3;
+    dev_gemm(HROW, GPJW, GPJB, XB, GTD, 2048, 512, nb*64,
+             kcb*512, kcb*512+512, kcb == 0, 1, 0, sA, sB);
+  }
+  gsync(bar, 448);
+  if (bid < 8) {
+    int nb = bid & 3, kcb = bid >> 2;
+    dev_gemm(GTD, BTW, BTB, nullptr, HBB, 512, 256, nb*64,
+             kcb*256, kcb*256+256, kcb == 0, 1, 0, sA, sB);
+  }
+  gsync(bar, 512);
+  if (bid == 0) {
+    float p0 = 0.f, p1 = 0.f;
+    for (int i = tid; i < 16384; i += 256) {
+      float h = HBB[i];
+      p0 = fmaf(h, CLW[i], p0);
+      p1 = fmaf(h, CLW[16384 + i], p1);
+    }
+    p0 = block_sum256(p0);
+    p1 = block_sum256(p1);
+    if (tid == 0) {
+      float l0 = p0 + CLB[0], l1 = p1 + CLB[1];
+      out[0] = l0; out[1] = l1;
+      out[2] = 1.f / (1.f + __expf(-l0));
+      out[3] = 1.f / (1.f + __expf(-l1));
+      out[4] = (l1 > l0) ? 1.f : 0.f;
+      float aux = 0.f;
+      for (int i = 0; i < 16; i++) aux += (SSUM[i] * (1.f / 64.f)) * ((float)CNT[i] * (1.f / 64.f));
+      out[5] = aux * 4.f * 0.01f;
+    }
+  }
+  if (bid == 1 && tid < 8) out[O_F2P + tid] = 0.f;
 }
 
 extern "C" void kernel_launch(void* const* d_in, const int* in_sizes, int n_in,
@@ -662,6 +776,7 @@
   float* BUF  = ws + OFF_BUF;
   float* SSUM = ws + OFF_SSUM;
   int*   CNT  = (int*)(ws + OFF_CNT);
+  unsigned* BAR = (unsigned*)(ws + OFF_BAR);
   float* Q    = ws + OFF_Q;
   float* AP   = ws + OFF_AP;
   float* QF   = ws + OFF_QF;
@@ -687,27 +802,14 @@
   bf16*  WL   = (bf16*)(ws + OFF_WL);
   float* YEXP = ws + OFF_YEXP;
 
-  k_zero<<<(ZERO_N + 255) / 256, 256, 0, stream>>>(ws, ZERO_N);
-  k_cvt_a<<<LNUM * NSEQ, 64, 0, stream>>>(SF, LN1G, LN1B, AH, AL);
-  k_cvt_w<<<LNUM * 1024, 64, 0, stream>>>(QKVW, WH, WL);
-  k_mfma_kv<<<dim3(32, 8, LNUM), 256, 0, stream>>>(AH, AL, WH, WL, QKVB, KT, VT);
-  k_ln<<<dim3(TTOK, LNUM), 64, 0, stream>>>(TOK, LN2G, LN2B, AOSH, 512);
-  k_gemm64<<<dim3(8, 4, LNUM), 256, 0, stream>>>(AOSH, QKVW, QKVB, nullptr, Q, 512, 512, 1536L*512, 1536, 0);
+  k_mega1<<<NZB + 4096 + 1024 + 64, 256, 0, stream>>>(
+      SF, LN1G, LN1B, QKVW, TOK, LN2G, LN2B, AH, AL, WH, WL, AOSH, ws);
+  k_l2<<<1024 + 128, 256, 0, stream>>>(AH, AL, WH, WL, QKVB, QKVW, AOSH, KT, VT, Q);
   k_attn<<<dim3(512, LNUM), 256, 0, stream>>>(KT, VT, Q, AOSH);
-  k_gemm64<<<dim3(8, 4, LNUM), 256, 0, stream>>>(AOSH, OUTW, OUTB, nullptr, AP, 512, 512, 512L*512, 512, 0);
-  k_gemm64<<<dim3(8, 4, LNUM), 256, 0, stream>>>(AP, MLPW, MLPB, nullptr, QF, 512, 512, 512L*512, 512, 0);
-  k_gemm64t<<<dim3(4, 4, LNUM), 256, 0, stream>>>(QF, GPW, P, 512, 256);
-  k_moe_gate<<<LNUM, 256, 0, stream>>>(P, GSIM, GTMP, QF, GATE, EXPI, POSI, KEEPI, SSUM, CNT, BUF);
-  k_moe_h<<<dim3(8, 16), 256, 0, stream>>>(BUF, EW1, EB1, HEXP);
-  k_moe_y<<<dim3(8, 16), 256, 0, stream>>>(HEXP, EW2, EB2, YEXP);
-  k_combine<<<TTOK, 512, 0, stream>>>(YEXP, EXPI, POSI, KEEPI, GATE, out + O_F1, out + O_F2, CUR);
-  k_ln<<<dim3(TTOK, 1), 64, 0, stream>>>(CUR, GL1G, GL1B, AOSH, 0);
-  k_gemm64<<<dim3(24, 4, 1), 256, 0, stream>>>(AOSH, GQKVW, GQKVB, nullptr, QKV3, 512, 1536, 0, 0, 0);
-  k_gsa_attn<<<8, 256, 0, stream>>>(QKV3, AO2);
-  k_gemm64<<<dim3(8, 4, 1), 256, 0, stream>>>(AO2, GOUTW, GOUTB, CUR, XB, 512, 512, 0, 0, 0);
-  k_ln<<<dim3(TTOK, 1), 64, 0, stream>>>(XB, GL2G, GL2B, AOSH, 0);
-  k_gemm64<<<dim3(32, 1, 1), 256, 0, stream>>>(AOSH, GFCW, GFCB, nullptr, HROW, 512, 2048, 0, 0, 1);
-  k_gemm64<<<dim3(8, 16, 1), 256, 0, stream>>>(HROW, GPJW, GPJB, XB, GTD, 2048, 512, 0, 0, 0);
-  k_gemm64<<<dim3(4, 4, 1), 256, 0, stream>>>(GTD, BTW, BTB, nullptr, HBB, 512, 256, 0, 0, 0);
-  k_final<<<1, 256, 0, stream>>>(HBB, CLW, CLB, SSUM, CNT, out);
-}
+  k_mega2<<<128, 256, 0, stream>>>(AOSH, OUTW, OUTB, AP, MLPW, MLPB, QF, GPW, P,
+      GSIM, GTMP, GATE, EXPI, POSI, KEEPI, SSUM, CNT, BUF,
+      EW1, EB1, HEXP, EW2, EB2, YEXP, out + O_F1, out + O_F2, CUR, BAR);
+  k_mega3<<<64, 256, 0, stream>>>(CUR, GL1G, GL1B, AOSH, GQKVW, GQKVB, QKV3, AO2,
+      GOUTW, GOUTB, XB, GL2G, GL2B, GFCW, GFCB, HROW,
+      GPJW, GPJB, GTD, BTW, BTB, HBB, CLW, CLB, SSUM, CNT, out, BAR + 1);
+}
```
